# Optimization experiments

Hardware: AMD Instinct MI355X
Metric: run time of the kernel (lower is better)

Reference implementation:

```python
import jax, jax.numpy as jnp
import numpy as np

D = 256; NH = 8; HD = D // NH; FF = 1024; NLAYERS = 6
REG_MAX = 32; NBIN = REG_MAX + 1; NC = 80; KQ = 4
SPATIAL = [(80, 80), (40, 40), (20, 20)]; NPTS = [4, 4, 4]; SUMP = sum(NPTS)
LQ = 300; B = 16; OFFSET_SCALE = 0.5; UP = 0.5; REG_SCALE = 4.0
TOT = NH * SUMP


def _project_np():
    ub1 = abs(UP) * abs(REG_SCALE); ub2 = ub1 * 2
    step = (ub1 + 1.0) ** (2.0 / (REG_MAX - 2))
    left = [-(step ** i) + 1 for i in range(REG_MAX // 2 - 1, 0, -1)]
    right = [step ** i - 1 for i in range(1, REG_MAX // 2)]
    return np.array([-ub2] + left + [0.0] + right + [ub2], dtype=np.float32)

PROJ_NP = _project_np()  # [NBIN]


def layer_norm(x, g, b):
    mu = x.mean(-1, keepdims=True)
    var = ((x - mu) ** 2).mean(-1, keepdims=True)
    return (x - mu) * jax.lax.rsqrt(var + 1e-5) * g + b


def inv_sigmoid(x, eps=1e-5):
    x = jnp.clip(x, eps, 1.0 - eps)
    return jnp.log(x) - jnp.log1p(-x)


def mlp2(x, w1, b1, w2, b2):
    return jax.nn.silu(x @ w1 + b1) @ w2 + b2


def mlp3(x, w1, b1, w2, b2, w3, b3):
    return jax.nn.silu(jax.nn.silu(x @ w1 + b1) @ w2 + b2) @ w3 + b3


def grid_sample(img, grid):
    # bilinear, padding_mode='zeros', align_corners=False. img [N,C,H,W], grid [N,Hg,Wg,2] in [-1,1]
    N, C, H, W = img.shape
    gshape = grid.shape[1:3]
    x = (grid[..., 0] + 1.0) * (W * 0.5) - 0.5
    y = (grid[..., 1] + 1.0) * (H * 0.5) - 0.5
    x0f = jnp.floor(x); y0f = jnp.floor(y)
    wx = x - x0f; wy = y - y0f
    x0 = x0f.astype(jnp.int32); y0 = y0f.astype(jnp.int32)
    imgf = img.reshape(N, C, H * W)
    def tap(xi, yi, wt):
        valid = ((xi >= 0) & (xi < W) & (yi >= 0) & (yi < H)).astype(img.dtype)
        idx = jnp.clip(yi, 0, H - 1) * W + jnp.clip(xi, 0, W - 1)
        v = jnp.take_along_axis(imgf, idx.reshape(N, 1, -1), axis=2).reshape(N, C, gshape[0], gshape[1])
        return v * (valid * wt)[:, None]
    return (tap(x0, y0, (1 - wx) * (1 - wy)) + tap(x0 + 1, y0, wx * (1 - wy))
            + tap(x0, y0 + 1, (1 - wx) * wy) + tap(x0 + 1, y0 + 1, wx * wy))


def self_attention(q_in, k_in, v_in, qw, qb, kw, kb, vw, vb, ow, ob):
    q = (q_in @ qw + qb).reshape(B, LQ, NH, HD)
    k = (k_in @ kw + kb).reshape(B, LQ, NH, HD)
    v = (v_in @ vw + vb).reshape(B, LQ, NH, HD)
    a = jax.nn.softmax(jnp.einsum('bqhd,bkhd->bhqk', q, k) * (HD ** -0.5), -1)
    o = jnp.einsum('bhqk,bkhd->bqhd', a, v).reshape(B, LQ, D)
    return o @ ow + ob


def distance2bbox(points, distance):
    rs = abs(REG_SCALE); half = 0.5 * rs
    x1 = points[..., 0] - (half + distance[..., 0]) * (points[..., 2] / rs)
    y1 = points[..., 1] - (half + distance[..., 1]) * (points[..., 3] / rs)
    x2 = points[..., 0] + (half + distance[..., 2]) * (points[..., 2] / rs)
    y2 = points[..., 1] + (half + distance[..., 3]) * (points[..., 3] / rs)
    return jnp.stack([(x1 + x2) * 0.5, (y1 + y2) * 0.5, x2 - x1, y2 - y1], -1)


def lqe_head(scores, corners, w1, b1, w2, b2):
    prob = jax.nn.softmax(corners.reshape(B, LQ, 4, NBIN), -1)
    topk, _ = jax.lax.top_k(prob, KQ)                         # [B,LQ,4,KQ]
    stat = jnp.concatenate([topk, topk.mean(-1, keepdims=True)], -1)  # [B,LQ,4,KQ+1]
    return scores + mlp2(stat.reshape(B, LQ, 4 * (KQ + 1)), w1, b1, w2, b2)


def reference(target, ref_pts_unact, memory,
              sa_qw, sa_qb, sa_kw, sa_kb, sa_vw, sa_vb, sa_ow, sa_ob,
              n1_g, n1_b, off_w, off_b, aw_w, aw_b,
              gate_w, gate_b, gn_g, gn_b,
              ff1_w, ff1_b, ff2_w, ff2_b, n3_g, n3_b,
              bb_w1, bb_b1, bb_w2, bb_b2, bb_w3, bb_b3,
              sc_w, sc_b, lqe_w1, lqe_b1, lqe_w2, lqe_b2,
              qp_w1, qp_b1, qp_w2, qp_b2,
              pb_w1, pb_b1, pb_w2, pb_b2, pb_w3, pb_b3):
    project = jnp.asarray(PROJ_NP)
    # --- value prep: memory [B,S,D] -> per-level [B*NH, HD, h, w] ---
    val = memory.reshape(B, -1, NH, HD).transpose(0, 2, 3, 1).reshape(B * NH, HD, -1)
    splits = np.cumsum([h * w for h, w in SPATIAL])[:-1].tolist()
    value_lvls = [v.reshape(B * NH, HD, h, w)
                  for v, (h, w) in zip(jnp.split(val, splits, axis=2), SPATIAL)]
    nps = jnp.asarray(np.repeat(1.0 / np.array(NPTS, np.float32), NPTS))  # [SUMP]

    ref_pts = jax.nn.sigmoid(ref_pts_unact)
    output = target
    out_prev = jnp.zeros_like(target)
    corners_prev = jnp.zeros((B, LQ, 4 * NBIN), dtype=target.dtype)
    ref_init = ref_pts
    final_logits = final_bboxes = None

    for i in range(NLAYERS):
        qp = jnp.clip(mlp2(ref_pts, qp_w1, qp_b1, qp_w2, qp_b2), -10.0, 10.0)
        # self attention
        q = output + qp
        t2 = self_attention(q, q, output, sa_qw[i], sa_qb[i], sa_kw[i], sa_kb[i],
                            sa_vw[i], sa_vb[i], sa_ow[i], sa_ob[i])
        output = layer_norm(output + t2, n1_g[i], n1_b[i])
        # deformable cross attention
        qc = output + qp
        offs = (qc @ off_w[i] + off_b[i]).reshape(B, LQ, NH, SUMP, 2)
        attnw = jax.nn.softmax((qc @ aw_w[i] + aw_b[i]).reshape(B, LQ, NH, SUMP), -1)
        offset = offs * nps[:, None] * ref_pts[:, :, None, None, 2:] * OFFSET_SCALE
        locs = ref_pts[:, :, None, None, :2] + offset            # [B,LQ,NH,SUMP,2]
        grids = (2.0 * locs - 1.0).transpose(0, 2, 1, 3, 4).reshape(B * NH, LQ, SUMP, 2)
        p0 = 0; sampled = []
        for lvl in range(len(SPATIAL)):
            sampled.append(grid_sample(value_lvls[lvl], grids[:, :, p0:p0 + NPTS[lvl]]))
            p0 += NPTS[lvl]
        samp = jnp.concatenate(sampled, -1)                      # [B*NH, HD, LQ, SUMP]
        aw = attnw.transpose(0, 2, 1, 3).reshape(B * NH, 1, LQ, SUMP)
        t2 = (samp * aw).sum(-1).reshape(B, D, LQ).transpose(0, 2, 1)
        # gateway
        g12 = jax.nn.sigmoid(jnp.concatenate([output, t2], -1) @ gate_w[i] + gate_b[i])
        output = layer_norm(g12[..., :D] * output + g12[..., D:] * t2, gn_g[i], gn_b[i])
        # FFN
        t2 = jax.nn.relu(output @ ff1_w[i] + ff1_b[i]) @ ff2_w[i] + ff2_b[i]
        output = layer_norm(jnp.clip(output + t2, -65504.0, 65504.0), n3_g[i], n3_b[i])
        # FDR box refinement
        if i == 0:
            pre_bb = jax.nn.sigmoid(mlp3(output, pb_w1, pb_b1, pb_w2, pb_b2, pb_w3, pb_b3)
                                    + inv_sigmoid(ref_pts))
            ref_init = pre_bb
        corners = mlp3(output + out_prev, bb_w1[i], bb_b1[i], bb_w2[i], bb_b2[i],
                       bb_w3[i], bb_b3[i]) + corners_prev
        dist = jax.nn.softmax(corners.reshape(B, LQ, 4, NBIN), -1) @ project  # [B,LQ,4]
        inter = distance2bbox(ref_init, dist)
        if i == NLAYERS - 1:  # eval_idx
            scores = output @ sc_w[i] + sc_b[i]
            final_logits = lqe_head(scores, corners, lqe_w1[i], lqe_b1[i], lqe_w2[i], lqe_b2[i])
            final_bboxes = inter
        corners_prev = corners
        ref_pts = inter
        out_prev = output
    return jnp.concatenate([final_bboxes, final_logits], -1)  # [B, LQ, 4+NC]


def setup_inputs() -> dict:
    key = jax.random.key(0)
    cnt = [0]
    def rnd(shape, scale=0.02):
        cnt[0] += 1
        return jax.random.normal(jax.random.fold_in(key, cnt[0]), shape, dtype=jnp.float32) * scale
    S = sum(h * w for h, w in SPATIAL)
    L = NLAYERS
    return {
        'target': rnd((B, LQ, D), 1.0),
        'ref_pts_unact': rnd((B, LQ, 4), 1.0),
        'memory': rnd((B, S, D), 1.0),
        'sa_qw': rnd((L, D, D)), 'sa_qb': rnd((L, D)),
        'sa_kw': rnd((L, D, D)), 'sa_kb': rnd((L, D)),
        'sa_vw': rnd((L, D, D)), 'sa_vb': rnd((L, D)),
        'sa_ow': rnd((L, D, D)), 'sa_ob': rnd((L, D)),
        'n1_g': jnp.ones((L, D)), 'n1_b': jnp.zeros((L, D)),
        'off_w': rnd((L, D, TOT * 2)), 'off_b': rnd((L, TOT * 2)),
        'aw_w': rnd((L, D, TOT)), 'aw_b': rnd((L, TOT)),
        'gate_w': rnd((L, 2 * D, 2 * D)), 'gate_b': rnd((L, 2 * D)),
        'gn_g': jnp.ones((L, D)), 'gn_b': jnp.zeros((L, D)),
        'ff1_w': rnd((L, D, FF)), 'ff1_b': rnd((L, FF)),
        'ff2_w': rnd((L, FF, D)), 'ff2_b': rnd((L, D)),
        'n3_g': jnp.ones((L, D)), 'n3_b': jnp.zeros((L, D)),
        'bb_w1': rnd((L, D, D)), 'bb_b1': rnd((L, D)),
        'bb_w2': rnd((L, D, D)), 'bb_b2': rnd((L, D)),
        'bb_w3': rnd((L, D, 4 * NBIN)), 'bb_b3': rnd((L, 4 * NBIN)),
        'sc_w': rnd((L, D, NC)), 'sc_b': rnd((L, NC)),
        'lqe_w1': rnd((L, 4 * (KQ + 1), 64)), 'lqe_b1': rnd((L, 64)),
        'lqe_w2': rnd((L, 64, 1)), 'lqe_b2': rnd((L, 1)),
        'qp_w1': rnd((4, 2 * D)), 'qp_b1': rnd((2 * D,)),
        'qp_w2': rnd((2 * D, D)), 'qp_b2': rnd((D,)),
        'pb_w1': rnd((D, D)), 'pb_b1': rnd((D,)),
        'pb_w2': rnd((D, D)), 'pb_b2': rnd((D,)),
        'pb_w3': rnd((D, 4)), 'pb_b3': rnd((4,)),
    }
```

## Files before the change

kernel.cpp:

```cpp
#include <hip/hip_runtime.h>
#include <cstddef>
#include <cmath>
#include <utility>

#define B_ 16
#define LQ_ 300
#define D_ 256
#define NH_ 8
#define HD_ 32
#define FF_ 1024
#define NBIN_ 33
#define NC_ 80
#define SUMP_ 12
#define TOT_ (NH_*SUMP_)
#define STOT_ 8400
#define R_ (B_*LQ_)
#define NLAYERS_ 6

typedef short bf16x8 __attribute__((ext_vector_type(8)));
typedef float f32x4  __attribute__((ext_vector_type(4)));

static __device__ __forceinline__ short f2bf(float x) {
  union { float f; unsigned u; } v; v.f = x;
  unsigned r = v.u + 0x7fffu + ((v.u >> 16) & 1u);
  return (short)(r >> 16);
}
static __device__ __forceinline__ float bf2f(short s) {
  union { unsigned u; float f; } v; v.u = ((unsigned)(unsigned short)s) << 16; return v.f;
}

struct WJob { const float* src; short* dst; int K, N, tk, tn, L, ostride, blk0, pad; };
struct WJobs { WJob j[17]; int njobs; };

__launch_bounds__(256)
__global__ void wconv_all(WJobs P) {
  __shared__ float t[32][33];
  const int b = blockIdx.x;
  int ji = 0;
  for (int k = 1; k < P.njobs; ++k) ji = (b >= P.j[k].blk0) ? k : ji;
  const float* src = P.j[ji].src;
  short* dst = P.j[ji].dst;
  const int K = P.j[ji].K, N = P.j[ji].N, tk = P.j[ji].tk;
  int rel = b - P.j[ji].blk0;
  int per = tk * P.j[ji].tn;
  int l = rel / per; int r2 = rel - l * per;
  int tki = r2 % tk, tni = r2 / tk;
  const float* Wl = src + (size_t)l * K * N;
  short* Wtl = dst + (size_t)l * (size_t)P.j[ji].ostride;
  int k0 = tki * 32, n0 = tni * 32;
  int tr = threadIdx.x >> 5, tc = threadIdx.x & 31;
  #pragma unroll
  for (int i = 0; i < 4; ++i) {
    int k = k0 + tr + i * 8, n = n0 + tc;
    t[tr + i * 8][tc] = (k < K && n < N) ? Wl[(size_t)k * N + n] : 0.f;
  }
  __syncthreads();
  #pragma unroll
  for (int i = 0; i < 4; ++i) {
    int n = n0 + tr + i * 8, k = k0 + tc;
    if (n < N && k < K) Wtl[(size_t)n * K + k] = f2bf(t[tc][tr + i * 8]);
  }
}

__launch_bounds__(256)
__global__ void memconv_kernel(const float* __restrict__ mem, short* __restrict__ mb) {
  int gs = blockIdx.x * 4 + (threadIdx.x >> 6);
  int c  = (threadIdx.x & 63) * 4;
  int b = gs / STOT_, s = gs - b * STOT_;
  float4 v = *(const float4*)(mem + (size_t)gs * 256 + c);
  int h = c >> 5, cc = c & 31;
  short4 o; o.x = f2bf(v.x); o.y = f2bf(v.y); o.z = f2bf(v.z); o.w = f2bf(v.w);
  *(short4*)(mb + (((size_t)(b * 8 + h) * STOT_ + s) * 32) + cc) = o;
}

__launch_bounds__(256)
__global__ void misc_init(const float* __restrict__ target, const float* __restrict__ refu,
                          const float* __restrict__ qb, const float* __restrict__ kb,
                          const float* __restrict__ vb, const float* __restrict__ ob,
                          const float* __restrict__ ab,
                          float* __restrict__ output, short* __restrict__ outbf,
                          float* __restrict__ out_prev, float* __restrict__ cprev,
                          float* __restrict__ refcur, float* __restrict__ qkvb,
                          float* __restrict__ offawb) {
  int i = blockIdx.x * 256 + threadIdx.x;
  float4 z; z.x = 0.f; z.y = 0.f; z.z = 0.f; z.w = 0.f;
  if (i < R_ * 64) {
    float4 v = ((const float4*)target)[i];
    ((float4*)output)[i] = v;
    short4 s; s.x = f2bf(v.x); s.y = f2bf(v.y); s.z = f2bf(v.z); s.w = f2bf(v.w);
    ((short4*)outbf)[i] = s;
    ((float4*)out_prev)[i] = z;
  }
  if (i < R_ * 33) ((float4*)cprev)[i] = z;
  if (i < R_) {
    float4 r = ((const float4*)refu)[i];
    float4 o;
    o.x = 1.f / (1.f + __expf(-r.x)); o.y = 1.f / (1.f + __expf(-r.y));
    o.z = 1.f / (1.f + __expf(-r.z)); o.w = 1.f / (1.f + __expf(-r.w));
    ((float4*)refcur)[i] = o;
  }
  if (i < NLAYERS_ * 768) {
    int l = i / 768, c = i % 768;
    qkvb[i] = (c < 256) ? qb[l * 256 + c] : (c < 512) ? kb[l * 256 + c - 256]
                        : vb[l * 256 + c - 512];
  }
  if (i < NLAYERS_ * 288) {
    int l = i / 288, c = i % 288;
    offawb[i] = (c < 192) ? ob[l * 192 + c] : ab[l * 96 + c - 192];
  }
}

__launch_bounds__(512)
__global__ void qp_qkv(const float* __restrict__ ref, const float* __restrict__ W1,
                       const float* __restrict__ b1, const short* __restrict__ W2t,
                       const float* __restrict__ b2, const float* __restrict__ output,
                       const short* __restrict__ outbf,
                       const short* __restrict__ Qt, const float* __restrict__ qkvbias,
                       float* __restrict__ qpout, short* __restrict__ qkvout) {
  __shared__ short sh[16 * 520];
  __shared__ short oqs[16][264];
  const int m0 = blockIdx.x * 16;
  const int tid = threadIdx.x;
  for (int i = tid; i < 16 * 512; i += 512) {
    int r = i >> 9, n = i & 511;
    float4 rv = *(const float4*)(ref + (size_t)(m0 + r) * 4);
    float v = b1[n] + rv.x * W1[n] + rv.y * W1[512 + n] + rv.z * W1[1024 + n]
            + rv.w * W1[1536 + n];
    v = v / (1.f + __expf(-v));
    sh[r * 520 + n] = f2bf(v);
  }
  __syncthreads();
  const int wid = tid >> 6, lane = tid & 63;
  const int lr = lane & 15, lq = lane >> 4;
  {
    f32x4 acc[2];
    acc[0] = (f32x4){0.f, 0.f, 0.f, 0.f};
    acc[1] = (f32x4){0.f, 0.f, 0.f, 0.f};
    #pragma unroll 4
    for (int k0 = 0; k0 < 512; k0 += 32) {
      bf16x8 a = *(const bf16x8*)&sh[lr * 520 + k0 + lq * 8];
      #pragma unroll
      for (int t = 0; t < 2; ++t) {
        bf16x8 w = *(const bf16x8*)(W2t + (size_t)(wid * 32 + t * 16 + lr) * 512 + k0 + lq * 8);
        acc[t] = __builtin_amdgcn_mfma_f32_16x16x32_bf16(a, w, acc[t], 0, 0, 0);
      }
    }
    #pragma unroll
    for (int t = 0; t < 2; ++t) {
      int col = wid * 32 + t * 16 + lr;
      float bv = b2[col];
      #pragma unroll
      for (int rr = 0; rr < 4; ++rr) {
        int rl = lq * 4 + rr;
        size_t idx = (size_t)(m0 + rl) * 256 + col;
        float v = fminf(fmaxf(acc[t][rr] + bv, -10.f), 10.f);
        qpout[idx] = v;
        oqs[rl][col] = f2bf(v + output[idx]);
      }
    }
  }
  __syncthreads();
  {
    f32x4 acc[6];
    #pragma unroll
    for (int t = 0; t < 6; ++t) acc[t] = (f32x4){0.f, 0.f, 0.f, 0.f};
    const int cbase = wid * 96;
    const short* obp = outbf + (size_t)(m0 + lr) * 256;
    #pragma unroll 2
    for (int k0 = 0; k0 < 256; k0 += 32) {
      bf16x8 a_oq = *(const bf16x8*)&oqs[lr][k0 + lq * 8];
      bf16x8 a_ob = *(const bf16x8*)(obp + k0 + lq * 8);
      #pragma unroll
      for (int t = 0; t < 6; ++t) {
        bf16x8 w = *(const bf16x8*)(Qt + (size_t)(cbase + t * 16 + lr) * 256 + k0 + lq * 8);
        acc[t] = __builtin_amdgcn_mfma_f32_16x16x32_bf16(
            (cbase + t * 16 < 512) ? a_oq : a_ob, w, acc[t], 0, 0, 0);
      }
    }
    #pragma unroll
    for (int t = 0; t < 6; ++t) {
      int colt = cbase + t * 16 + lr;
      float bv = qkvbias[colt];
      #pragma unroll
      for (int rr = 0; rr < 4; ++rr)
        qkvout[(size_t)(m0 + lq * 4 + rr) * 768 + colt] = f2bf(acc[t][rr] + bv);
    }
  }
}

__launch_bounds__(512)
__global__ void sow_ln_off(const short* __restrict__ A, const short* __restrict__ Wt,
                           const float* __restrict__ bias, const float* __restrict__ resid,
                           const float* __restrict__ gamma, const float* __restrict__ beta,
                           const float* __restrict__ qp,
                           const short* __restrict__ OWt, const float* __restrict__ ob,
                           float* __restrict__ outf, short* __restrict__ outbf,
                           float* __restrict__ offout) {
  __shared__ float ssum[16][8];
  __shared__ float ssq[16][8];
  __shared__ short oqs[16][264];
  const int m0 = blockIdx.x * 16;
  const int tid = threadIdx.x, wid = tid >> 6, lane = tid & 63;
  const int lr = lane & 15, lq = lane >> 4;
  const int arow = m0 + lr;
  const int cw = wid * 32;
  f32x4 acc[2];
  acc[0] = (f32x4){0.f, 0.f, 0.f, 0.f};
  acc[1] = (f32x4){0.f, 0.f, 0.f, 0.f};
  #pragma unroll 4
  for (int k0 = 0; k0 < 256; k0 += 32) {
    bf16x8 a = *(const bf16x8*)(A + (size_t)arow * 256 + k0 + lq * 8);
    #pragma unroll
    for (int t = 0; t < 2; ++t) {
      bf16x8 w = *(const bf16x8*)(Wt + (size_t)(cw + t * 16 + lr) * 256 + k0 + lq * 8);
      acc[t] = __builtin_amdgcn_mfma_f32_16x16x32_bf16(a, w, acc[t], 0, 0, 0);
    }
  }
  float s[4] = {0.f, 0.f, 0.f, 0.f}, q[4] = {0.f, 0.f, 0.f, 0.f};
  #pragma unroll
  for (int t = 0; t < 2; ++t) {
    int col = cw + t * 16 + lr;
    float bv = bias[col];
    #pragma unroll
    for (int rr = 0; rr < 4; ++rr) {
      int rowg = m0 + lq * 4 + rr;
      float x = acc[t][rr] + bv + resid[(size_t)rowg * 256 + col];
      acc[t][rr] = x;
      s[rr] += x; q[rr] += x * x;
    }
  }
  #pragma unroll
  for (int m = 1; m < 16; m <<= 1)
    #pragma unroll
    for (int rr = 0; rr < 4; ++rr) { s[rr] += __shfl_xor(s[rr], m); q[rr] += __shfl_xor(q[rr], m); }
  if (lr == 0)
    #pragma unroll
    for (int rr = 0; rr < 4; ++rr) {
      ssum[lq * 4 + rr][wid] = s[rr];
      ssq[lq * 4 + rr][wid] = q[rr];
    }
  __syncthreads();
  float mu[4], rs[4];
  #pragma unroll
  for (int rr = 0; rr < 4; ++rr) {
    int rl = lq * 4 + rr;
    float sm = 0.f, sq = 0.f;
    #pragma unroll
    for (int w8 = 0; w8 < 8; ++w8) { sm += ssum[rl][w8]; sq += ssq[rl][w8]; }
    float m_ = sm * (1.f / 256.f);
    float var = sq * (1.f / 256.f) - m_ * m_;
    mu[rr] = m_; rs[rr] = rsqrtf(var + 1e-5f);
  }
  #pragma unroll
  for (int t = 0; t < 2; ++t) {
    int col = cw + t * 16 + lr;
    float g = gamma[col], be = beta[col];
    #pragma unroll
    for (int rr = 0; rr < 4; ++rr) {
      int rl = lq * 4 + rr;
      size_t idx = (size_t)(m0 + rl) * 256 + col;
      float v = (acc[t][rr] - mu[rr]) * rs[rr] * g + be;
      outf[idx] = v;
      outbf[idx] = f2bf(v);
      oqs[rl][col] = f2bf(v + qp[idx]);
    }
  }
  __syncthreads();
  f32x4 oacc[3];
  #pragma unroll
  for (int j = 0; j < 3; ++j) oacc[j] = (f32x4){0.f, 0.f, 0.f, 0.f};
  #pragma unroll 2
  for (int k0 = 0; k0 < 256; k0 += 32) {
    bf16x8 a = *(const bf16x8*)&oqs[lr][k0 + lq * 8];
    #pragma unroll
    for (int j = 0; j < 3; ++j) {
      int tile = wid + j * 8;
      int trow = (tile < 18) ? tile * 16 + lr : 0;
      bf16x8 w = *(const bf16x8*)(OWt + (size_t)trow * 256 + k0 + lq * 8);
      oacc[j] = __builtin_amdgcn_mfma_f32_16x16x32_bf16(a, w, oacc[j], 0, 0, 0);
    }
  }
  #pragma unroll
  for (int j = 0; j < 3; ++j) {
    int tile = wid + j * 8;
    if (tile >= 18) continue;
    int col = tile * 16 + lr;
    float bv = ob[col];
    #pragma unroll
    for (int rr = 0; rr < 4; ++rr)
      offout[(size_t)(m0 + lq * 4 + rr) * 288 + col] = oacc[j][rr] + bv;
  }
}

template<int SCORES>
__launch_bounds__(512)
__global__ void ffn_ln(const short* __restrict__ A, const short* __restrict__ W1t,
                       const float* __restrict__ b1, const short* __restrict__ W2t,
                       const float* __restrict__ b2, const float* __restrict__ resid,
                       const float* __restrict__ gamma, const float* __restrict__ beta,
                       float* __restrict__ prev, float* __restrict__ outf,
                       short* __restrict__ outbf, short* __restrict__ oqbf,
                       const short* __restrict__ SCt, const float* __restrict__ scb,
                       float* __restrict__ scoresOut) {
  __shared__ short hid[16][1032];
  __shared__ float ssum[16][8];
  __shared__ float ssq[16][8];
  const int m0 = blockIdx.x * 16;
  const int tid = threadIdx.x, wid = tid >> 6, lane = tid & 63;
  const int lr = lane & 15, lq = lane >> 4;
  const int arow = m0 + lr;
  {
    f32x4 acc[8];
    #pragma unroll
    for (int t = 0; t < 8; ++t) acc[t] = (f32x4){0.f, 0.f, 0.f, 0.f};
    #pragma unroll 2
    for (int k0 = 0; k0 < 256; k0 += 32) {
      bf16x8 a = *(const bf16x8*)(A + (size_t)arow * 256 + k0 + lq * 8);
      #pragma unroll
      for (int t = 0; t < 8; ++t) {
        bf16x8 w = *(const bf16x8*)(W1t + (size_t)(wid * 128 + t * 16 + lr) * 256 + k0 + lq * 8);
        acc[t] = __builtin_amdgcn_mfma_f32_16x16x32_bf16(a, w, acc[t], 0, 0, 0);
      }
    }
    #pragma unroll
    for (int t = 0; t < 8; ++t) {
      int col = wid * 128 + t * 16 + lr;
      float bv = b1[col];
      #pragma unroll
      for (int rr = 0; rr < 4; ++rr)
        hid[lq * 4 + rr][col] = f2bf(fmaxf(acc[t][rr] + bv, 0.f));
    }
  }
  __syncthreads();
  const int cw = wid * 32;
  f32x4 acc[2];
  acc[0] = (f32x4){0.f, 0.f, 0.f, 0.f};
  acc[1] = (f32x4){0.f, 0.f, 0.f, 0.f};
  #pragma unroll 4
  for (int k0 = 0; k0 < 1024; k0 += 32) {
    bf16x8 a = *(const bf16x8*)&hid[lr][k0 + lq * 8];
    #pragma unroll
    for (int t = 0; t < 2; ++t) {
      bf16x8 w = *(const bf16x8*)(W2t + (size_t)(cw + t * 16 + lr) * 1024 + k0 + lq * 8);
      acc[t] = __builtin_amdgcn_mfma_f32_16x16x32_bf16(a, w, acc[t], 0, 0, 0);
    }
  }
  float s[4] = {0.f, 0.f, 0.f, 0.f}, q[4] = {0.f, 0.f, 0.f, 0.f};
  #pragma unroll
  for (int t = 0; t < 2; ++t) {
    int col = cw + t * 16 + lr;
    float bv = b2[col];
    #pragma unroll
    for (int rr = 0; rr < 4; ++rr) {
      int rowg = m0 + lq * 4 + rr;
      float x = acc[t][rr] + bv + resid[(size_t)rowg * 256 + col];
      x = fminf(fmaxf(x, -65504.f), 65504.f);
      acc[t][rr] = x;
      s[rr] += x; q[rr] += x * x;
    }
  }
  #pragma unroll
  for (int m = 1; m < 16; m <<= 1)
    #pragma unroll
    for (int rr = 0; rr < 4; ++rr) { s[rr] += __shfl_xor(s[rr], m); q[rr] += __shfl_xor(q[rr], m); }
  if (lr == 0)
    #pragma unroll
    for (int rr = 0; rr < 4; ++rr) {
      ssum[lq * 4 + rr][wid] = s[rr];
      ssq[lq * 4 + rr][wid] = q[rr];
    }
  __syncthreads();
  float mu[4], rs[4];
  #pragma unroll
  for (int rr = 0; rr < 4; ++rr) {
    int rl = lq * 4 + rr;
    float sm = 0.f, sq = 0.f;
    #pragma unroll
    for (int w8 = 0; w8 < 8; ++w8) { sm += ssum[rl][w8]; sq += ssq[rl][w8]; }
    float m_ = sm * (1.f / 256.f);
    float var = sq * (1.f / 256.f) - m_ * m_;
    mu[rr] = m_; rs[rr] = rsqrtf(var + 1e-5f);
  }
  #pragma unroll
  for (int t = 0; t < 2; ++t) {
    int col = cw + t * 16 + lr;
    float g = gamma[col], be = beta[col];
    #pragma unroll
    for (int rr = 0; rr < 4; ++rr) {
      int rl = lq * 4 + rr;
      size_t idx = (size_t)(m0 + rl) * 256 + col;
      float v = (acc[t][rr] - mu[rr]) * rs[rr] * g + be;
      outf[idx] = v;
      short vb = f2bf(v);
      outbf[idx] = vb;
      float po = prev[idx];
      oqbf[idx] = f2bf(v + po);
      prev[idx] = v;
      if (SCORES) hid[rl][col] = vb;
    }
  }
  if (SCORES) {
    __syncthreads();
    f32x4 sacc = (f32x4){0.f, 0.f, 0.f, 0.f};
    int trow = (wid < 5) ? wid * 16 + lr : 0;
    #pragma unroll 2
    for (int k0 = 0; k0 < 256; k0 += 32) {
      bf16x8 a = *(const bf16x8*)&hid[lr][k0 + lq * 8];
      bf16x8 w = *(const bf16x8*)(SCt + (size_t)trow * 256 + k0 + lq * 8);
      sacc = __builtin_amdgcn_mfma_f32_16x16x32_bf16(a, w, sacc, 0, 0, 0);
    }
    if (wid < 5) {
      int col = wid * 16 + lr;
      float bv = scb[col];
      #pragma unroll
      for (int rr = 0; rr < 4; ++rr)
        scoresOut[(size_t)(m0 + lq * 4 + rr) * 80 + col] = sacc[rr] + bv;
    }
  }
}

template<int LQE>
__launch_bounds__(512)
__global__ void fdr_kernel(const short* __restrict__ A,
                           const short* __restrict__ W1t, const float* __restrict__ b1,
                           const short* __restrict__ W2t, const float* __restrict__ b2,
                           const short* __restrict__ W3t, const float* __restrict__ b3,
                           const float* __restrict__ cprev, const float* __restrict__ refi,
                           float* __restrict__ ccur, float* __restrict__ refn,
                           const float* __restrict__ scores, const float* __restrict__ lw1,
                           const float* __restrict__ lb1, const float* __restrict__ lw2,
                           const float* __restrict__ lb2, float* __restrict__ outp) {
  __shared__ short h1[16][264];
  __shared__ short h2[16][264];
  __shared__ float cor[16][132];
  __shared__ float dstl[16][4];
  __shared__ float projs[33];
  __shared__ float statl[16][20];
  __shared__ float interb[16][4];
  __shared__ float lqes[16];
  const int m0 = blockIdx.x * 16;
  const int tid = threadIdx.x, wid = tid >> 6, lane = tid & 63;
  const int lr = lane & 15, lq = lane >> 4;
  if (tid < 33) {
    float v;
    if (tid == 0) v = -4.f;
    else if (tid == 32) v = 4.f;
    else if (tid == 16) v = 0.f;
    else if (tid < 16) v = 1.f - powf(3.f, (float)(16 - tid) * (1.f / 15.f));
    else v = powf(3.f, (float)(tid - 16) * (1.f / 15.f)) - 1.f;
    projs[tid] = v;
  }
  {
    f32x4 acc[2];
    acc[0] = (f32x4){0.f, 0.f, 0.f, 0.f};
    acc[1] = (f32x4){0.f, 0.f, 0.f, 0.f};
    #pragma unroll 2
    for (int k0 = 0; k0 < 256; k0 += 32) {
      bf16x8 a = *(const bf16x8*)(A + (size_t)(m0 + lr) * 256 + k0 + lq * 8);
      #pragma unroll
      for (int t = 0; t < 2; ++t) {
        bf16x8 w = *(const bf16x8*)(W1t + (size_t)(wid * 32 + t * 16 + lr) * 256 + k0 + lq * 8);
        acc[t] = __builtin_amdgcn_mfma_f32_16x16x32_bf16(a, w, acc[t], 0, 0, 0);
      }
    }
    #pragma unroll
    for (int t = 0; t < 2; ++t) {
      int col = wid * 32 + t * 16 + lr;
      float bv = b1[col];
      #pragma unroll
      for (int rr = 0; rr < 4; ++rr) {
        float v = acc[t][rr] + bv;
        v = v / (1.f + __expf(-v));
        h1[lq * 4 + rr][col] = f2bf(v);
      }
    }
  }
  __syncthreads();
  {
    f32x4 acc[2];
    acc[0] = (f32x4){0.f, 0.f, 0.f, 0.f};
    acc[1] = (f32x4){0.f, 0.f, 0.f, 0.f};
    #pragma unroll 2
    for (int k0 = 0; k0 < 256; k0 += 32) {
      bf16x8 a = *(const bf16x8*)&h1[lr][k0 + lq * 8];
      #pragma unroll
      for (int t = 0; t < 2; ++t) {
        bf16x8 w = *(const bf16x8*)(W2t + (size_t)(wid * 32 + t * 16 + lr) * 256 + k0 + lq * 8);
        acc[t] = __builtin_amdgcn_mfma_f32_16x16x32_bf16(a, w, acc[t], 0, 0, 0);
      }
    }
    #pragma unroll
    for (int t = 0; t < 2; ++t) {
      int col = wid * 32 + t * 16 + lr;
      float bv = b2[col];
      #pragma unroll
      for (int rr = 0; rr < 4; ++rr) {
        float v = acc[t][rr] + bv;
        v = v / (1.f + __expf(-v));
        h2[lq * 4 + rr][col] = f2bf(v);
      }
    }
  }
  __syncthreads();
  {
    f32x4 acc[2];
    int col[2], wr[2];
    #pragma unroll
    for (int j = 0; j < 2; ++j) {
      acc[j] = (f32x4){0.f, 0.f, 0.f, 0.f};
      col[j] = (wid + j * 8) * 16 + lr;
      wr[j] = (col[j] < 132) ? col[j] : 0;
    }
    #pragma unroll 2
    for (int k0 = 0; k0 < 256; k0 += 32) {
      bf16x8 a = *(const bf16x8*)&h2[lr][k0 + lq * 8];
      #pragma unroll
      for (int j = 0; j < 2; ++j) {
        bf16x8 w = *(const bf16x8*)(W3t + (size_t)wr[j] * 256 + k0 + lq * 8);
        acc[j] = __builtin_amdgcn_mfma_f32_16x16x32_bf16(a, w, acc[j], 0, 0, 0);
      }
    }
    #pragma unroll
    for (int j = 0; j < 2; ++j) {
      if (col[j] >= 132) continue;
      float bv = b3[col[j]];
      #pragma unroll
      for (int rr = 0; rr < 4; ++rr) {
        int rl = lq * 4 + rr, g = m0 + rl;
        float v = acc[j][rr] + bv + cprev[(size_t)g * 132 + col[j]];
        ccur[(size_t)g * 132 + col[j]] = v;
        cor[rl][col[j]] = v;
      }
    }
  }
  __syncthreads();
  if (tid < 64) {
    int r = tid >> 2, sd = tid & 3;
    const float* cp = &cor[r][sd * 33];
    float m = -1e30f;
    #pragma unroll
    for (int j = 0; j < 33; ++j) m = fmaxf(m, cp[j]);
    float t0 = -1e30f, t1 = -1e30f, t2v = -1e30f, t3 = -1e30f;
    float sum = 0.f, dot = 0.f;
    #pragma unroll
    for (int j = 0; j < 33; ++j) {
      float e = __expf(cp[j] - m);
      sum += e; dot += e * projs[j];
      if (LQE) {
        if (e > t0)      { t3 = t2v; t2v = t1; t1 = t0; t0 = e; }
        else if (e > t1) { t3 = t2v; t2v = t1; t1 = e; }
        else if (e > t2v){ t3 = t2v; t2v = e; }
        else if (e > t3) { t3 = e; }
      }
    }
    dstl[r][sd] = dot / sum;
    if (LQE) {
      float inv = 1.f / sum;
      float v0 = t0 * inv, v1 = t1 * inv, v2 = t2v * inv, v3 = t3 * inv;
      statl[r][sd * 5 + 0] = v0; statl[r][sd * 5 + 1] = v1;
      statl[r][sd * 5 + 2] = v2; statl[r][sd * 5 + 3] = v3;
      statl[r][sd * 5 + 4] = (v0 + v1 + v2 + v3) * 0.25f;
    }
  }
  __syncthreads();
  if (tid < 16) {
    int g = m0 + tid;
    float px = refi[g * 4], py = refi[g * 4 + 1];
    float qw = refi[g * 4 + 2] * 0.25f, qh = refi[g * 4 + 3] * 0.25f;
    float x1 = px - (2.f + dstl[tid][0]) * qw, y1 = py - (2.f + dstl[tid][1]) * qh;
    float x2 = px + (2.f + dstl[tid][2]) * qw, y2 = py + (2.f + dstl[tid][3]) * qh;
    float4 o; o.x = (x1 + x2) * 0.5f; o.y = (y1 + y2) * 0.5f; o.z = x2 - x1; o.w = y2 - y1;
    *(float4*)(refn + (size_t)g * 4) = o;
    if (LQE) { interb[tid][0] = o.x; interb[tid][1] = o.y; interb[tid][2] = o.z; interb[tid][3] = o.w; }
  }
  if (LQE) {
    #pragma unroll
    for (int it = 0; it < 2; ++it) {
      int row = wid * 2 + it;
      float sv = lb1[lane];
      #pragma unroll
      for (int i = 0; i < 20; ++i) sv += statl[row][i] * lw1[i * 64 + lane];
      float hv = sv / (1.f + __expf(-sv));
      float v = hv * lw2[lane];
      #pragma unroll
      for (int o = 32; o; o >>= 1) v += __shfl_xor(v, o);
      if (lane == 0) lqes[row] = v + lb2[0];
    }
    __syncthreads();
    for (int idx = tid; idx < 16 * 84; idx += 512) {
      int r = idx / 84, c = idx - r * 84;
      int g = m0 + r;
      outp[(size_t)g * 84 + c] = (c < 4) ? interb[r][c]
                                         : scores[(size_t)g * 80 + (c - 4)] + lqes[r];
    }
  }
}

__launch_bounds__(512)
__global__ void pb_fused(const short* __restrict__ A,
                         const short* __restrict__ W1t, const float* __restrict__ b1,
                         const short* __restrict__ W2t, const float* __restrict__ b2,
                         const short* __restrict__ W3t, const float* __restrict__ b3,
                         const float* __restrict__ refc, float* __restrict__ refinit) {
  __shared__ short h1[16][264];
  __shared__ short h2[16][264];
  const int m0 = blockIdx.x * 16;
  const int tid = threadIdx.x, wid = tid >> 6, lane = tid & 63;
  const int lr = lane & 15, lq = lane >> 4;
  {
    f32x4 acc[2];
    acc[0] = (f32x4){0.f, 0.f, 0.f, 0.f};
    acc[1] = (f32x4){0.f, 0.f, 0.f, 0.f};
    #pragma unroll 2
    for (int k0 = 0; k0 < 256; k0 += 32) {
      bf16x8 a = *(const bf16x8*)(A + (size_t)(m0 + lr) * 256 + k0 + lq * 8);
      #pragma unroll
      for (int t = 0; t < 2; ++t) {
        bf16x8 w = *(const bf16x8*)(W1t + (size_t)(wid * 32 + t * 16 + lr) * 256 + k0 + lq * 8);
        acc[t] = __builtin_amdgcn_mfma_f32_16x16x32_bf16(a, w, acc[t], 0, 0, 0);
      }
    }
    #pragma unroll
    for (int t = 0; t < 2; ++t) {
      int col = wid * 32 + t * 16 + lr;
      float bv = b1[col];
      #pragma unroll
      for (int rr = 0; rr < 4; ++rr) {
        float v = acc[t][rr] + bv;
        v = v / (1.f + __expf(-v));
        h1[lq * 4 + rr][col] = f2bf(v);
      }
    }
  }
  __syncthreads();
  {
    f32x4 acc[2];
    acc[0] = (f32x4){0.f, 0.f, 0.f, 0.f};
    acc[1] = (f32x4){0.f, 0.f, 0.f, 0.f};
    #pragma unroll 2
    for (int k0 = 0; k0 < 256; k0 += 32) {
      bf16x8 a = *(const bf16x8*)&h1[lr][k0 + lq * 8];
      #pragma unroll
      for (int t = 0; t < 2; ++t) {
        bf16x8 w = *(const bf16x8*)(W2t + (size_t)(wid * 32 + t * 16 + lr) * 256 + k0 + lq * 8);
        acc[t] = __builtin_amdgcn_mfma_f32_16x16x32_bf16(a, w, acc[t], 0, 0, 0);
      }
    }
    #pragma unroll
    for (int t = 0; t < 2; ++t) {
      int col = wid * 32 + t * 16 + lr;
      float bv = b2[col];
      #pragma unroll
      for (int rr = 0; rr < 4; ++rr) {
        float v = acc[t][rr] + bv;
        v = v / (1.f + __expf(-v));
        h2[lq * 4 + rr][col] = f2bf(v);
      }
    }
  }
  __syncthreads();
  if (wid == 0) {
    f32x4 acc = (f32x4){0.f, 0.f, 0.f, 0.f};
    const short* wp = W3t + (size_t)((lr < 4) ? lr : 0) * 256;
    #pragma unroll 2
    for (int k0 = 0; k0 < 256; k0 += 32) {
      bf16x8 a = *(const bf16x8*)&h2[lr][k0 + lq * 8];
      bf16x8 w = *(const bf16x8*)(wp + k0 + lq * 8);
      acc = __builtin_amdgcn_mfma_f32_16x16x32_bf16(a, w, acc, 0, 0, 0);
    }
    if (lr < 4) {
      float bv = b3[lr];
      #pragma unroll
      for (int rr = 0; rr < 4; ++rr) {
        int g = m0 + lq * 4 + rr;
        float pre = acc[rr] + bv;
        float x = fminf(fmaxf(refc[(size_t)g * 4 + lr], 1e-5f), 1.f - 1e-5f);
        float is = logf(x) - log1pf(-x);
        refinit[(size_t)g * 4 + lr] = 1.f / (1.f + __expf(-(pre + is)));
      }
    }
  }
}

__launch_bounds__(512)
__global__ void gate_ln(const short* __restrict__ Abf, const short* __restrict__ tbf,
                        const short* __restrict__ Wt, const float* __restrict__ bias,
                        const float* __restrict__ t2,
                        const float* __restrict__ gamma, const float* __restrict__ beta,
                        float* __restrict__ output, short* __restrict__ outbf) {
  __shared__ float sg[16][520];
  const int m0 = blockIdx.x * 16;
  const int tid = threadIdx.x, wid = tid >> 6, lane = tid & 63;
  const int lr = lane & 15, lq = lane >> 4;
  const int arow = m0 + lr;
  f32x4 acc[4];
  #pragma unroll
  for (int t = 0; t < 4; ++t) acc[t] = (f32x4){0.f, 0.f, 0.f, 0.f};
  #pragma unroll 2
  for (int k0 = 0; k0 < 512; k0 += 32) {
    const short* src = (k0 < 256) ? Abf : tbf;
    int ko = (k0 < 256) ? k0 : k0 - 256;
    bf16x8 a = *(const bf16x8*)(src + (size_t)arow * 256 + ko + lq * 8);
    #pragma unroll
    for (int t = 0; t < 4; ++t) {
      bf16x8 w = *(const bf16x8*)(Wt + (size_t)(wid * 64 + t * 16 + lr) * 512 + k0 + lq * 8);
      acc[t] = __builtin_amdgcn_mfma_f32_16x16x32_bf16(a, w, acc[t], 0, 0, 0);
    }
  }
  #pragma unroll
  for (int t = 0; t < 4; ++t) {
    int col = wid * 64 + t * 16 + lr;
    float bv = bias[col];
    #pragma unroll
    for (int rr = 0; rr < 4; ++rr) {
      int rl = lq * 4 + rr;
      sg[rl][col] = 1.f / (1.f + __expf(-(acc[t][rr] + bv)));
    }
  }
  __syncthreads();
  #pragma unroll
  for (int it = 0; it < 2; ++it) {
    int rl = wid + it * 8;
    int rowg = m0 + rl;
    int c = lane * 4;
    float4 o4 = *(const float4*)(output + (size_t)rowg * 256 + c);
    float4 t4 = *(const float4*)(t2 + (size_t)rowg * 256 + c);
    float4 g1 = *(const float4*)&sg[rl][c];
    float4 g2 = *(const float4*)&sg[rl][256 + c];
    float x0 = g1.x * o4.x + g2.x * t4.x;
    float x1 = g1.y * o4.y + g2.y * t4.y;
    float x2 = g1.z * o4.z + g2.z * t4.z;
    float x3 = g1.w * o4.w + g2.w * t4.w;
    float s = x0 + x1 + x2 + x3;
    float q = x0 * x0 + x1 * x1 + x2 * x2 + x3 * x3;
    #pragma unroll
    for (int o = 32; o; o >>= 1) { s += __shfl_xor(s, o); q += __shfl_xor(q, o); }
    float mu = s * (1.f / 256.f);
    float var = q * (1.f / 256.f) - mu * mu;
    float rs = rsqrtf(var + 1e-5f);
    float4 ga = *(const float4*)(gamma + c);
    float4 be = *(const float4*)(beta + c);
    float v0 = (x0 - mu) * rs * ga.x + be.x;
    float v1 = (x1 - mu) * rs * ga.y + be.y;
    float v2 = (x2 - mu) * rs * ga.z + be.z;
    float v3 = (x3 - mu) * rs * ga.w + be.w;
    float4 vo; vo.x = v0; vo.y = v1; vo.z = v2; vo.w = v3;
    *(float4*)(output + (size_t)rowg * 256 + c) = vo;
    short4 vs; vs.x = f2bf(v0); vs.y = f2bf(v1); vs.z = f2bf(v2); vs.w = f2bf(v3);
    *(short4*)(outbf + (size_t)rowg * 256 + c) = vs;
  }
}

__launch_bounds__(256)
__global__ void attn3_kernel(const short* __restrict__ qkv, short* __restrict__ O) {
  __shared__ short Kb[304][40];
  __shared__ short Vt[32][328];
  __shared__ short Pw[4][16][328];
  const int half = blockIdx.x & 1, bh = blockIdx.x >> 1;
  const int h = bh & 7, b = bh >> 3;
  const int tid = threadIdx.x;
  const short* QKVb = qkv + (size_t)b * LQ_ * 768;
  for (int idx = tid; idx < 304 * 4; idx += 256) {
    int row = idx >> 2, seg = (idx & 3) * 8;
    bf16x8 v = (row < 300) ? *(const bf16x8*)(QKVb + (size_t)row * 768 + 256 + h * 32 + seg)
                           : (bf16x8){0,0,0,0,0,0,0,0};
    *(bf16x8*)&Kb[row][seg] = v;
  }
  for (int idx = tid; idx < 300 * 4; idx += 256) {
    int row = idx >> 2, seg = (idx & 3) * 8;
    bf16x8 v = *(const bf16x8*)(QKVb + (size_t)row * 768 + 512 + h * 32 + seg);
    #pragma unroll
    for (int j = 0; j < 8; ++j) Vt[seg + j][row] = v[j];
  }
  for (int idx = tid; idx < 32 * 20; idx += 256) Vt[idx / 20][300 + idx % 20] = 0;
  for (int idx = tid; idx < 4 * 16 * 16; idx += 256)
    Pw[idx >> 8][(idx >> 4) & 15][304 + (idx & 15)] = 0;
  __syncthreads();

  const int wid = tid >> 6, lane = tid & 63;
  const int lr = lane & 15, lq = lane >> 4;
  short (*Pl)[328] = Pw[wid];
  const float scale = 0.17677669529663687f;

  for (int qt = wid; qt < 10; qt += 4) {
    const int q0 = half * 150 + qt * 16;
    int qrow = q0 + lr; if (qrow > 299) qrow = 299;
    bf16x8 af_q = *(const bf16x8*)(QKVb + (size_t)qrow * 768 + h * 32 + lq * 8);
    f32x4 s[19];
    #pragma unroll
    for (int t = 0; t < 19; ++t) {
      bf16x8 bk = *(const bf16x8*)&Kb[t * 16 + lr][lq * 8];
      s[t] = __builtin_amdgcn_mfma_f32_16x16x32_bf16(af_q, bk, (f32x4){0.f,0.f,0.f,0.f}, 0, 0, 0);
    }
    #pragma unroll
    for (int t = 0; t < 19; ++t)
      #pragma unroll
      for (int r = 0; r < 4; ++r) s[t][r] *= scale;
    if (lr >= 12) { s[18][0] = s[18][1] = s[18][2] = s[18][3] = -1e30f; }
    float l[4];
    #pragma unroll
    for (int r = 0; r < 4; ++r) {
      float mm = -1e30f;
      #pragma unroll
      for (int t = 0; t < 19; ++t) mm = fmaxf(mm, s[t][r]);
      #pragma unroll
      for (int x = 1; x < 16; x <<= 1) mm = fmaxf(mm, __shfl_xor(mm, x));
      float ll = 0.f;
      #pragma unroll
      for (int t = 0; t < 19; ++t) { float p = __expf(s[t][r] - mm); s[t][r] = p; ll += p; }
      #pragma unroll
      for (int x = 1; x < 16; x <<= 1) ll += __shfl_xor(ll, x);
      l[r] = ll;
    }
    #pragma unroll
    for (int t = 0; t < 19; ++t)
      #pragma unroll
      for (int r = 0; r < 4; ++r) Pl[lq * 4 + r][t * 16 + lr] = f2bf(s[t][r]);
    f32x4 o0 = (f32x4){0.f,0.f,0.f,0.f}, o1 = (f32x4){0.f,0.f,0.f,0.f};
    #pragma unroll
    for (int c = 0; c < 10; ++c) {
      bf16x8 ap = *(const bf16x8*)&Pl[lr][c * 32 + lq * 8];
      bf16x8 v0 = *(const bf16x8*)&Vt[lr][c * 32 + lq * 8];
      bf16x8 v1 = *(const bf16x8*)&Vt[16 + lr][c * 32 + lq * 8];
      o0 = __builtin_amdgcn_mfma_f32_16x16x32_bf16(ap, v0, o0, 0, 0, 0);
      o1 = __builtin_amdgcn_mfma_f32_16x16x32_bf16(ap, v1, o1, 0, 0, 0);
    }
    #pragma unroll
    for (int r = 0; r < 4; ++r) {
      int q = q0 + lq * 4 + r;
      if (q >= 300) continue;
      float inv = 1.f / l[r];
      size_t ob = (size_t)(b * LQ_ + q) * 256 + h * 32;
      O[ob + lr]      = f2bf(o0[r] * inv);
      O[ob + 16 + lr] = f2bf(o1[r] * inv);
    }
  }
}

template<int BF16MEM>
__launch_bounds__(256)
__global__ void deform_kernel(const void* __restrict__ memv, const float* __restrict__ offaw,
                              const float* __restrict__ refp,
                              float* __restrict__ t2, short* __restrict__ t2bf) {
  const int bi = blockIdx.x;
  const int row = (bi & 7) * 600 + (bi >> 3);
  const int b = row / LQ_;
  const int tid = threadIdx.x;
  const int h = tid >> 5, c = tid & 31;
  const float rx = refp[row * 4 + 0], ry = refp[row * 4 + 1];
  const float rw = refp[row * 4 + 2], rh = refp[row * 4 + 3];
  const float* awp = offaw + (size_t)row * 288 + 192 + h * SUMP_;
  float wv[SUMP_];
  float wmax = -1e30f;
  #pragma unroll
  for (int p = 0; p < SUMP_; ++p) { wv[p] = awp[p]; wmax = fmaxf(wmax, wv[p]); }
  float wsum = 0.f;
  #pragma unroll
  for (int p = 0; p < SUMP_; ++p) { wv[p] = __expf(wv[p] - wmax); wsum += wv[p]; }
  const float winv = 1.f / wsum;
  const float* op = offaw + (size_t)row * 288 + h * (SUMP_ * 2);
  const short* mb16 = BF16MEM ? ((const short*)memv + ((size_t)(b * 8 + h) * STOT_) * 32 + c) : nullptr;
  const float* mb32 = BF16MEM ? nullptr : ((const float*)memv + (size_t)b * STOT_ * 256 + h * 32 + c);
  float acc = 0.f;
  #pragma unroll
  for (int p = 0; p < SUMP_; ++p) {
    const int lvl = p >> 2;
    const int Wl = (lvl == 0) ? 80 : ((lvl == 1) ? 40 : 20);
    const int s0 = (lvl == 0) ? 0 : ((lvl == 1) ? 6400 : 8000);
    float lx = rx + op[2 * p]     * 0.125f * rw;
    float ly = ry + op[2 * p + 1] * 0.125f * rh;
    float x = lx * Wl - 0.5f, y = ly * Wl - 0.5f;
    float xf = floorf(x), yf = floorf(y);
    int x0 = (int)xf, y0 = (int)yf;
    float wx = x - xf, wy = y - yf;
    int x0c = min(max(x0, 0), Wl - 1), x1c = min(max(x0 + 1, 0), Wl - 1);
    int y0c = min(max(y0, 0), Wl - 1), y1c = min(max(y0 + 1, 0), Wl - 1);
    float wx0 = (x0 >= 0 && x0 < Wl) ? (1.f - wx) : 0.f;
    float wx1 = (x0 + 1 >= 0 && x0 + 1 < Wl) ? wx : 0.f;
    float wy0 = (y0 >= 0 && y0 < Wl) ? (1.f - wy) : 0.f;
    float wy1 = (y0 + 1 >= 0 && y0 + 1 < Wl) ? wy : 0.f;
    float v;
    if (BF16MEM) {
      const short* mb = mb16 + (size_t)s0 * 32;
      v = wx0 * wy0 * bf2f(mb[(size_t)(y0c * Wl + x0c) * 32])
        + wx1 * wy0 * bf2f(mb[(size_t)(y0c * Wl + x1c) * 32])
        + wx0 * wy1 * bf2f(mb[(size_t)(y1c * Wl + x0c) * 32])
        + wx1 * wy1 * bf2f(mb[(size_t)(y1c * Wl + x1c) * 32]);
    } else {
      const float* mb = mb32 + (size_t)s0 * 256;
      v = wx0 * wy0 * mb[(size_t)(y0c * Wl + x0c) * 256]
        + wx1 * wy0 * mb[(size_t)(y0c * Wl + x1c) * 256]
        + wx0 * wy1 * mb[(size_t)(y1c * Wl + x0c) * 256]
        + wx1 * wy1 * mb[(size_t)(y1c * Wl + x1c) * 256];
    }
    acc += wv[p] * winv * v;
  }
  size_t off = (size_t)row * D_ + h * HD_ + c;
  t2[off] = acc;
  t2bf[off] = f2bf(acc);
}

static inline dim3 egrid(int n) { return dim3((n + 255) / 256); }

extern "C" void kernel_launch(void* const* d_in, const int* in_sizes, int n_in,
                              void* d_out, int out_size, void* d_ws, size_t ws_size,
                              hipStream_t stream) {
  const float* target     = (const float*)d_in[0];
  const float* ref_unact  = (const float*)d_in[1];
  const float* memory     = (const float*)d_in[2];
  const float* sa_qw = (const float*)d_in[3];  const float* sa_qb = (const float*)d_in[4];
  const float* sa_kw = (const float*)d_in[5];  const float* sa_kb = (const float*)d_in[6];
  const float* sa_vw = (const float*)d_in[7];  const float* sa_vb = (const float*)d_in[8];
  const float* sa_ow = (const float*)d_in[9];  const float* sa_ob = (const float*)d_in[10];
  const float* n1_g  = (const float*)d_in[11]; const float* n1_b  = (const float*)d_in[12];
  const float* off_w = (const float*)d_in[13]; const float* off_b = (const float*)d_in[14];
  const float* aw_w  = (const float*)d_in[15]; const float* aw_b  = (const float*)d_in[16];
  const float* gate_w= (const float*)d_in[17]; const float* gate_b= (const float*)d_in[18];
  const float* gn_g  = (const float*)d_in[19]; const float* gn_b  = (const float*)d_in[20];
  const float* ff1_w = (const float*)d_in[21]; const float* ff1_b = (const float*)d_in[22];
  const float* ff2_w = (const float*)d_in[23]; const float* ff2_b = (const float*)d_in[24];
  const float* n3_g  = (const float*)d_in[25]; const float* n3_b  = (const float*)d_in[26];
  const float* bb_w1 = (const float*)d_in[27]; const float* bb_b1 = (const float*)d_in[28];
  const float* bb_w2 = (const float*)d_in[29]; const float* bb_b2 = (const float*)d_in[30];
  const float* bb_w3 = (const float*)d_in[31]; const float* bb_b3 = (const float*)d_in[32];
  const float* sc_w  = (const float*)d_in[33]; const float* sc_b  = (const float*)d_in[34];
  const float* lqe_w1= (const float*)d_in[35]; const float* lqe_b1= (const float*)d_in[36];
  const float* lqe_w2= (const float*)d_in[37]; const float* lqe_b2= (const float*)d_in[38];
  const float* qp_w1 = (const float*)d_in[39]; const float* qp_b1 = (const float*)d_in[40];
  const float* qp_w2 = (const float*)d_in[41]; const float* qp_b2 = (const float*)d_in[42];
  const float* pb_w1 = (const float*)d_in[43]; const float* pb_b1 = (const float*)d_in[44];
  const float* pb_w2 = (const float*)d_in[45]; const float* pb_b2 = (const float*)d_in[46];
  const float* pb_w3 = (const float*)d_in[47]; const float* pb_b3 = (const float*)d_in[48];
  float* out = (float*)d_out;

  float* ws = (float*)d_ws;
  size_t woff = 0;
  auto alloc = [&](size_t n) { float* p = ws + woff; woff += n; return p; };
  float* output   = alloc((size_t)R_ * D_);
  float* out_prev = alloc((size_t)R_ * D_);
  float* qp       = alloc((size_t)R_ * D_);
  float* t2       = alloc((size_t)R_ * D_);
  float* offawf   = alloc((size_t)R_ * 288);
  float* U        = alloc((size_t)R_ * 512);
  float* corners0 = alloc((size_t)R_ * 4 * NBIN_);
  float* corners1 = alloc((size_t)R_ * 4 * NBIN_);
  float* refA     = alloc((size_t)R_ * 4);
  float* refB     = alloc((size_t)R_ * 4);
  float* ref_init = alloc((size_t)R_ * 4);
  float* qkvb     = alloc((size_t)NLAYERS_ * 768);
  float* offawb   = alloc((size_t)NLAYERS_ * 288);

  short* sws = (short*)(ws + woff);
  size_t soff = 0;
  auto salloc = [&](size_t n) { short* p = sws + soff; soff += n; return p; };
  short* outbf = salloc((size_t)R_ * D_);
  short* oqbf  = salloc((size_t)R_ * D_);
  short* tbf   = salloc((size_t)R_ * D_);
  short* qp2t  = salloc((size_t)256 * 512);
  short* sqkvt = salloc((size_t)NLAYERS_ * 768 * 256);
  short* sowt  = salloc((size_t)NLAYERS_ * 256 * 256);
  short* soffawt = salloc((size_t)NLAYERS_ * 288 * 256);
  short* gatet = salloc((size_t)NLAYERS_ * 512 * 512);
  short* ff1t  = salloc((size_t)NLAYERS_ * 1024 * 256);
  short* ff2t  = salloc((size_t)NLAYERS_ * 256 * 1024);
  short* bb1t  = salloc((size_t)NLAYERS_ * 256 * 256);
  short* bb2t  = salloc((size_t)NLAYERS_ * 256 * 256);
  short* bb3t  = salloc((size_t)NLAYERS_ * 132 * 256);
  short* pb1t  = salloc((size_t)256 * 256);
  short* pb2t  = salloc((size_t)256 * 256);
  short* pb3t  = salloc((size_t)4 * 256);
  short* sct   = salloc((size_t)80 * 256);
  size_t base_bytes = woff * sizeof(float) + soff * sizeof(short);
  if (ws_size < base_bytes) return;
  const size_t memn = (size_t)B_ * STOT_ * 256;
  bool bf16mem = (ws_size >= base_bytes + memn * sizeof(short));
  short* membf = sws + soff;

  short* qkv    = (short*)U;
  float* scores = offawf;

  float* c_prev = corners0; float* c_cur = corners1;
  float* ref_cur = refA;    float* ref_nxt = refB;

  WJobs P; int nb = 0; int nj = 0;
  auto addj = [&](const float* s, short* d2, int K, int N, int L, int ostr) {
    P.j[nj].src = s; P.j[nj].dst = d2; P.j[nj].K = K; P.j[nj].N = N;
    P.j[nj].tk = (K + 31) / 32; P.j[nj].tn = (N + 31) / 32;
    P.j[nj].L = L; P.j[nj].ostride = ostr; P.j[nj].blk0 = nb; P.j[nj].pad = 0;
    nb += P.j[nj].tk * P.j[nj].tn * L; ++nj;
  };
  addj(qp_w2, qp2t, 512, 256, 1, 512 * 256);
  addj(sa_qw, sqkvt,               256, 256, NLAYERS_, 768 * 256);
  addj(sa_kw, sqkvt + 256 * 256,   256, 256, NLAYERS_, 768 * 256);
  addj(sa_vw, sqkvt + 512 * 256,   256, 256, NLAYERS_, 768 * 256);
  addj(sa_ow, sowt, 256, 256, NLAYERS_, 256 * 256);
  addj(off_w, soffawt,             256, 192, NLAYERS_, 288 * 256);
  addj(aw_w,  soffawt + 192 * 256, 256,  96, NLAYERS_, 288 * 256);
  addj(gate_w, gatet, 512, 512, NLAYERS_, 512 * 512);
  addj(ff1_w, ff1t, 256, 1024, NLAYERS_, 1024 * 256);
  addj(ff2_w, ff2t, 1024, 256, NLAYERS_, 256 * 1024);
  addj(bb_w1, bb1t, 256, 256, NLAYERS_, 256 * 256);
  addj(bb_w2, bb2t, 256, 256, NLAYERS_, 256 * 256);
  addj(bb_w3, bb3t, 256, 132, NLAYERS_, 132 * 256);
  addj(pb_w1, pb1t, 256, 256, 1, 256 * 256);
  addj(pb_w2, pb2t, 256, 256, 1, 256 * 256);
  addj(pb_w3, pb3t, 256, 4, 1, 4 * 256);
  addj(sc_w + (size_t)5 * D_ * NC_, sct, 256, 80, 1, 80 * 256);
  P.njobs = nj;
  wconv_all<<<dim3(nb), 256, 0, stream>>>(P);
  if (bf16mem)
    memconv_kernel<<<dim3(B_ * STOT_ / 4), 256, 0, stream>>>(memory, membf);

  misc_init<<<egrid(R_ * 64), 256, 0, stream>>>(target, ref_unact,
      sa_qb, sa_kb, sa_vb, off_b, aw_b,
      output, outbf, out_prev, c_prev, ref_cur, qkvb, offawb);

  for (int i = 0; i < NLAYERS_; ++i) {
    qp_qkv<<<dim3(300), 512, 0, stream>>>(ref_cur, qp_w1, qp_b1, qp2t, qp_b2,
                                          output, outbf,
                                          sqkvt + (size_t)i * 768 * 256,
                                          qkvb + (size_t)i * 768, qp, qkv);
    attn3_kernel<<<dim3(B_ * NH_ * 2), 256, 0, stream>>>(qkv, tbf);
    sow_ln_off<<<dim3(300), 512, 0, stream>>>(
        tbf, sowt + (size_t)i * 65536, sa_ob + (size_t)i * D_, output,
        n1_g + (size_t)i * D_, n1_b + (size_t)i * D_, qp,
        soffawt + (size_t)i * 288 * 256, offawb + (size_t)i * 288,
        output, outbf, offawf);

    if (bf16mem)
      deform_kernel<1><<<dim3(R_), 256, 0, stream>>>(membf, offawf, ref_cur, t2, tbf);
    else
      deform_kernel<0><<<dim3(R_), 256, 0, stream>>>(memory, offawf, ref_cur, t2, tbf);

    gate_ln<<<dim3(300), 512, 0, stream>>>(outbf, tbf, gatet + (size_t)i * 262144,
                                           gate_b + (size_t)i * 512, t2,
                                           gn_g + (size_t)i * D_, gn_b + (size_t)i * D_,
                                           output, outbf);

    if (i < NLAYERS_ - 1)
      ffn_ln<0><<<dim3(300), 512, 0, stream>>>(outbf, ff1t + (size_t)i * 262144,
          ff1_b + (size_t)i * FF_, ff2t + (size_t)i * 262144, ff2_b + (size_t)i * D_,
          output, n3_g + (size_t)i * D_, n3_b + (size_t)i * D_,
          out_prev, output, outbf, oqbf, nullptr, nullptr, nullptr);
    else
      ffn_ln<1><<<dim3(300), 512, 0, stream>>>(outbf, ff1t + (size_t)i * 262144,
          ff1_b + (size_t)i * FF_, ff2t + (size_t)i * 262144, ff2_b + (size_t)i * D_,
          output, n3_g + (size_t)i * D_, n3_b + (size_t)i * D_,
          out_prev, output, outbf, oqbf, sct, sc_b + (size_t)5 * NC_, scores);

    if (i == 0)
      pb_fused<<<dim3(300), 512, 0, stream>>>(outbf, pb1t, pb_b1, pb2t, pb_b2,
                                              pb3t, pb_b3, ref_cur, ref_init);
    if (i < NLAYERS_ - 1) {
      fdr_kernel<0><<<dim3(300), 512, 0, stream>>>(oqbf,
          bb1t + (size_t)i * 65536, bb_b1 + (size_t)i * D_,
          bb2t + (size_t)i * 65536, bb_b2 + (size_t)i * D_,
          bb3t + (size_t)i * 33792, bb_b3 + (size_t)i * 4 * NBIN_,
          c_prev, ref_init, c_cur, ref_nxt,
          nullptr, nullptr, nullptr, nullptr, nullptr, nullptr);
      std::swap(c_prev, c_cur);
      std::swap(ref_cur, ref_nxt);
    } else {
      fdr_kernel<1><<<dim3(300), 512, 0, stream>>>(oqbf,
          bb1t + (size_t)i * 65536, bb_b1 + (size_t)i * D_,
          bb2t + (size_t)i * 65536, bb_b2 + (size_t)i * D_,
          bb3t + (size_t)i * 33792, bb_b3 + (size_t)i * 4 * NBIN_,
          c_prev, ref_init, c_cur, ref_nxt,
          scores, lqe_w1 + (size_t)5 * 20 * 64, lqe_b1 + (size_t)5 * 64,
          lqe_w2 + (size_t)5 * 64, lqe_b2 + (size_t)5, out);
    }
  }
}
```

Measured before the change: 1.885 ms.

## Double row tile to 32 per block across fused GEMM kernels

Every fused MFMA kernel (qp_qkv, sow_ln_off, ffn_ln, gate_ln, pb_fused, fdr) now handles 32 rows per block instead of 16. Each weight fragment is reused for two A tiles, which halves global weight traffic per row. Grids drop from 300 to 150 blocks. The deform kernel also packs two rows per 512-thread block. The tradeoff is fewer blocks than the MI355X's CU count (256), more registers and LDS per block, and lower occupancy.

Result: faster. 1.607 ms (-14.8%).

```diff
diff --git a/kernel.cpp b/kernel.cpp
--- a/kernel.cpp
+++ b/kernel.cpp
@@ -117,11 +117,11 @@
                        const short* __restrict__ outbf,
                        const short* __restrict__ Qt, const float* __restrict__ qkvbias,
                        float* __restrict__ qpout, short* __restrict__ qkvout) {
-  __shared__ short sh[16 * 520];
-  __shared__ short oqs[16][264];
-  const int m0 = blockIdx.x * 16;
+  __shared__ short sh[32 * 520];
+  __shared__ short oqs[32][264];
+  const int m0 = blockIdx.x * 32;
   const int tid = threadIdx.x;
-  for (int i = tid; i < 16 * 512; i += 512) {
+  for (int i = tid; i < 32 * 512; i += 512) {
     int r = i >> 9, n = i & 511;
     float4 rv = *(const float4*)(ref + (size_t)(m0 + r) * 4);
     float v = b1[n] + rv.x * W1[n] + rv.y * W1[512 + n] + rv.z * W1[1024 + n]
@@ -133,16 +133,20 @@
   const int wid = tid >> 6, lane = tid & 63;
   const int lr = lane & 15, lq = lane >> 4;
   {
-    f32x4 acc[2];
-    acc[0] = (f32x4){0.f, 0.f, 0.f, 0.f};
-    acc[1] = (f32x4){0.f, 0.f, 0.f, 0.f};
+    f32x4 acc[2][2];
+    #pragma unroll
+    for (int ti = 0; ti < 2; ++ti)
+      #pragma unroll
+      for (int t = 0; t < 2; ++t) acc[ti][t] = (f32x4){0.f, 0.f, 0.f, 0.f};
     #pragma unroll 4
     for (int k0 = 0; k0 < 512; k0 += 32) {
-      bf16x8 a = *(const bf16x8*)&sh[lr * 520 + k0 + lq * 8];
+      bf16x8 a0 = *(const bf16x8*)&sh[lr * 520 + k0 + lq * 8];
+      bf16x8 a1 = *(const bf16x8*)&sh[(16 + lr) * 520 + k0 + lq * 8];
       #pragma unroll
       for (int t = 0; t < 2; ++t) {
         bf16x8 w = *(const bf16x8*)(W2t + (size_t)(wid * 32 + t * 16 + lr) * 512 + k0 + lq * 8);
-        acc[t] = __builtin_amdgcn_mfma_f32_16x16x32_bf16(a, w, acc[t], 0, 0, 0);
+        acc[0][t] = __builtin_amdgcn_mfma_f32_16x16x32_bf16(a0, w, acc[0][t], 0, 0, 0);
+        acc[1][t] = __builtin_amdgcn_mfma_f32_16x16x32_bf16(a1, w, acc[1][t], 0, 0, 0);
       }
     }
     #pragma unroll
@@ -150,31 +154,39 @@
       int col = wid * 32 + t * 16 + lr;
       float bv = b2[col];
       #pragma unroll
-      for (int rr = 0; rr < 4; ++rr) {
-        int rl = lq * 4 + rr;
-        size_t idx = (size_t)(m0 + rl) * 256 + col;
-        float v = fminf(fmaxf(acc[t][rr] + bv, -10.f), 10.f);
-        qpout[idx] = v;
-        oqs[rl][col] = f2bf(v + output[idx]);
-      }
+      for (int ti = 0; ti < 2; ++ti)
+        #pragma unroll
+        for (int rr = 0; rr < 4; ++rr) {
+          int rl = ti * 16 + lq * 4 + rr;
+          size_t idx = (size_t)(m0 + rl) * 256 + col;
+          float v = fminf(fmaxf(acc[ti][t][rr] + bv, -10.f), 10.f);
+          qpout[idx] = v;
+          oqs[rl][col] = f2bf(v + output[idx]);
+        }
     }
   }
   __syncthreads();
   {
-    f32x4 acc[6];
-    #pragma unroll
-    for (int t = 0; t < 6; ++t) acc[t] = (f32x4){0.f, 0.f, 0.f, 0.f};
+    f32x4 acc[2][6];
+    #pragma unroll
+    for (int ti = 0; ti < 2; ++ti)
+      #pragma unroll
+      for (int t = 0; t < 6; ++t) acc[ti][t] = (f32x4){0.f, 0.f, 0.f, 0.f};
     const int cbase = wid * 96;
-    const short* obp = outbf + (size_t)(m0 + lr) * 256;
+    const short* obp0 = outbf + (size_t)(m0 + lr) * 256;
+    const short* obp1 = outbf + (size_t)(m0 + 16 + lr) * 256;
     #pragma unroll 2
     for (int k0 = 0; k0 < 256; k0 += 32) {
-      bf16x8 a_oq = *(const bf16x8*)&oqs[lr][k0 + lq * 8];
-      bf16x8 a_ob = *(const bf16x8*)(obp + k0 + lq * 8);
+      bf16x8 aq0 = *(const bf16x8*)&oqs[lr][k0 + lq * 8];
+      bf16x8 aq1 = *(const bf16x8*)&oqs[16 + lr][k0 + lq * 8];
+      bf16x8 ab0 = *(const bf16x8*)(obp0 + k0 + lq * 8);
+      bf16x8 ab1 = *(const bf16x8*)(obp1 + k0 + lq * 8);
       #pragma unroll
       for (int t = 0; t < 6; ++t) {
         bf16x8 w = *(const bf16x8*)(Qt + (size_t)(cbase + t * 16 + lr) * 256 + k0 + lq * 8);
-        acc[t] = __builtin_amdgcn_mfma_f32_16x16x32_bf16(
-            (cbase + t * 16 < 512) ? a_oq : a_ob, w, acc[t], 0, 0, 0);
+        bool useoq = (cbase + t * 16) < 512;
+        acc[0][t] = __builtin_amdgcn_mfma_f32_16x16x32_bf16(useoq ? aq0 : ab0, w, acc[0][t], 0, 0, 0);
+        acc[1][t] = __builtin_amdgcn_mfma_f32_16x16x32_bf16(useoq ? aq1 : ab1, w, acc[1][t], 0, 0, 0);
       }
     }
     #pragma unroll
@@ -182,8 +194,10 @@
       int colt = cbase + t * 16 + lr;
       float bv = qkvbias[colt];
       #pragma unroll
-      for (int rr = 0; rr < 4; ++rr)
-        qkvout[(size_t)(m0 + lq * 4 + rr) * 768 + colt] = f2bf(acc[t][rr] + bv);
+      for (int ti = 0; ti < 2; ++ti)
+        #pragma unroll
+        for (int rr = 0; rr < 4; ++rr)
+          qkvout[(size_t)(m0 + ti * 16 + lq * 4 + rr) * 768 + colt] = f2bf(acc[ti][t][rr] + bv);
     }
   }
 }
@@ -196,88 +210,112 @@
                            const short* __restrict__ OWt, const float* __restrict__ ob,
                            float* __restrict__ outf, short* __restrict__ outbf,
                            float* __restrict__ offout) {
-  __shared__ float ssum[16][8];
-  __shared__ float ssq[16][8];
-  __shared__ short oqs[16][264];
-  const int m0 = blockIdx.x * 16;
+  __shared__ float ssum[32][8];
+  __shared__ float ssq[32][8];
+  __shared__ short oqs[32][264];
+  const int m0 = blockIdx.x * 32;
   const int tid = threadIdx.x, wid = tid >> 6, lane = tid & 63;
   const int lr = lane & 15, lq = lane >> 4;
-  const int arow = m0 + lr;
   const int cw = wid * 32;
-  f32x4 acc[2];
-  acc[0] = (f32x4){0.f, 0.f, 0.f, 0.f};
-  acc[1] = (f32x4){0.f, 0.f, 0.f, 0.f};
+  f32x4 acc[2][2];
+  #pragma unroll
+  for (int ti = 0; ti < 2; ++ti)
+    #pragma unroll
+    for (int t = 0; t < 2; ++t) acc[ti][t] = (f32x4){0.f, 0.f, 0.f, 0.f};
   #pragma unroll 4
   for (int k0 = 0; k0 < 256; k0 += 32) {
-    bf16x8 a = *(const bf16x8*)(A + (size_t)arow * 256 + k0 + lq * 8);
+    bf16x8 a0 = *(const bf16x8*)(A + (size_t)(m0 + lr) * 256 + k0 + lq * 8);
+    bf16x8 a1 = *(const bf16x8*)(A + (size_t)(m0 + 16 + lr) * 256 + k0 + lq * 8);
     #pragma unroll
     for (int t = 0; t < 2; ++t) {
       bf16x8 w = *(const bf16x8*)(Wt + (size_t)(cw + t * 16 + lr) * 256 + k0 + lq * 8);
-      acc[t] = __builtin_amdgcn_mfma_f32_16x16x32_bf16(a, w, acc[t], 0, 0, 0);
-    }
-  }
-  float s[4] = {0.f, 0.f, 0.f, 0.f}, q[4] = {0.f, 0.f, 0.f, 0.f};
+      acc[0][t] = __builtin_amdgcn_mfma_f32_16x16x32_bf16(a0, w, acc[0][t], 0, 0, 0);
+      acc[1][t] = __builtin_amdgcn_mfma_f32_16x16x32_bf16(a1, w, acc[1][t], 0, 0, 0);
+    }
+  }
+  float s[2][4], q[2][4];
+  #pragma unroll
+  for (int ti = 0; ti < 2; ++ti)
+    #pragma unroll
+    for (int rr = 0; rr < 4; ++rr) { s[ti][rr] = 0.f; q[ti][rr] = 0.f; }
   #pragma unroll
   for (int t = 0; t < 2; ++t) {
     int col = cw + t * 16 + lr;
     float bv = bias[col];
     #pragma unroll
+    for (int ti = 0; ti < 2; ++ti)
+      #pragma unroll
+      for (int rr = 0; rr < 4; ++rr) {
+        int rowg = m0 + ti * 16 + lq * 4 + rr;
+        float x = acc[ti][t][rr] + bv + resid[(size_t)rowg * 256 + col];
+        acc[ti][t][rr] = x;
+        s[ti][rr] += x; q[ti][rr] += x * x;
+      }
+  }
+  #pragma unroll
+  for (int m = 1; m < 16; m <<= 1)
+    #pragma unroll
+    for (int ti = 0; ti < 2; ++ti)
+      #pragma unroll
+      for (int rr = 0; rr < 4; ++rr) {
+        s[ti][rr] += __shfl_xor(s[ti][rr], m);
+        q[ti][rr] += __shfl_xor(q[ti][rr], m);
+      }
+  if (lr == 0)
+    #pragma unroll
+    for (int ti = 0; ti < 2; ++ti)
+      #pragma unroll
+      for (int rr = 0; rr < 4; ++rr) {
+        ssum[ti * 16 + lq * 4 + rr][wid] = s[ti][rr];
+        ssq[ti * 16 + lq * 4 + rr][wid] = q[ti][rr];
+      }
+  __syncthreads();
+  float mu[2][4], rs[2][4];
+  #pragma unroll
+  for (int ti = 0; ti < 2; ++ti)
+    #pragma unroll
     for (int rr = 0; rr < 4; ++rr) {
-      int rowg = m0 + lq * 4 + rr;
-      float x = acc[t][rr] + bv + resid[(size_t)rowg * 256 + col];
-      acc[t][rr] = x;
-      s[rr] += x; q[rr] += x * x;
-    }
-  }
-  #pragma unroll
-  for (int m = 1; m < 16; m <<= 1)
-    #pragma unroll
-    for (int rr = 0; rr < 4; ++rr) { s[rr] += __shfl_xor(s[rr], m); q[rr] += __shfl_xor(q[rr], m); }
-  if (lr == 0)
-    #pragma unroll
-    for (int rr = 0; rr < 4; ++rr) {
-      ssum[lq * 4 + rr][wid] = s[rr];
-      ssq[lq * 4 + rr][wid] = q[rr];
-    }
-  __syncthreads();
-  float mu[4], rs[4];
-  #pragma unroll
-  for (int rr = 0; rr < 4; ++rr) {
-    int rl = lq * 4 + rr;
-    float sm = 0.f, sq = 0.f;
-    #pragma unroll
-    for (int w8 = 0; w8 < 8; ++w8) { sm += ssum[rl][w8]; sq += ssq[rl][w8]; }
-    float m_ = sm * (1.f / 256.f);
-    float var = sq * (1.f / 256.f) - m_ * m_;
-    mu[rr] = m_; rs[rr] = rsqrtf(var + 1e-5f);
-  }
+      int rl = ti * 16 + lq * 4 + rr;
+      float sm = 0.f, sq = 0.f;
+      #pragma unroll
+      for (int w8 = 0; w8 < 8; ++w8) { sm += ssum[rl][w8]; sq += ssq[rl][w8]; }
+      float m_ = sm * (1.f / 256.f);
+      float var = sq * (1.f / 256.f) - m_ * m_;
+      mu[ti][rr] = m_; rs[ti][rr] = rsqrtf(var + 1e-5f);
+    }
   #pragma unroll
   for (int t = 0; t < 2; ++t) {
     int col = cw + t * 16 + lr;
     float g = gamma[col], be = beta[col];
     #pragma unroll
-    for (int rr = 0; rr < 4; ++rr) {
-      int rl = lq * 4 + rr;
-      size_t idx = (size_t)(m0 + rl) * 256 + col;
-      float v = (acc[t][rr] - mu[rr]) * rs[rr] * g + be;
-      outf[idx] = v;
-      outbf[idx] = f2bf(v);
-      oqs[rl][col] = f2bf(v + qp[idx]);
-    }
-  }
-  __syncthreads();
-  f32x4 oacc[3];
-  #pragma unroll
-  for (int j = 0; j < 3; ++j) oacc[j] = (f32x4){0.f, 0.f, 0.f, 0.f};
+    for (int ti = 0; ti < 2; ++ti)
+      #pragma unroll
+      for (int rr = 0; rr < 4; ++rr) {
+        int rl = ti * 16 + lq * 4 + rr;
+        size_t idx = (size_t)(m0 + rl) * 256 + col;
+        float v = (acc[ti][t][rr] - mu[ti][rr]) * rs[ti][rr] * g + be;
+        outf[idx] = v;
+        outbf[idx] = f2bf(v);
+        oqs[rl][col] = f2bf(v + qp[idx]);
+      }
+  }
+  __syncthreads();
+  f32x4 oacc[2][3];
+  #pragma unroll
+  for (int ti = 0; ti < 2; ++ti)
+    #pragma unroll
+    for (int j = 0; j < 3; ++j) oacc[ti][j] = (f32x4){0.f, 0.f, 0.f, 0.f};
   #pragma unroll 2
   for (int k0 = 0; k0 < 256; k0 += 32) {
-    bf16x8 a = *(const bf16x8*)&oqs[lr][k0 + lq * 8];
+    bf16x8 a0 = *(const bf16x8*)&oqs[lr][k0 + lq * 8];
+    bf16x8 a1 = *(const bf16x8*)&oqs[16 + lr][k0 + lq * 8];
     #pragma unroll
     for (int j = 0; j < 3; ++j) {
       int tile = wid + j * 8;
       int trow = (tile < 18) ? tile * 16 + lr : 0;
       bf16x8 w = *(const bf16x8*)(OWt + (size_t)trow * 256 + k0 + lq * 8);
-      oacc[j] = __builtin_amdgcn_mfma_f32_16x16x32_bf16(a, w, oacc[j], 0, 0, 0);
+      oacc[0][j] = __builtin_amdgcn_mfma_f32_16x16x32_bf16(a0, w, oacc[0][j], 0, 0, 0);
+      oacc[1][j] = __builtin_amdgcn_mfma_f32_16x16x32_bf16(a1, w, oacc[1][j], 0, 0, 0);
     }
   }
   #pragma unroll
@@ -287,8 +325,10 @@
     int col = tile * 16 + lr;
     float bv = ob[col];
     #pragma unroll
-    for (int rr = 0; rr < 4; ++rr)
-      offout[(size_t)(m0 + lq * 4 + rr) * 288 + col] = oacc[j][rr] + bv;
+    for (int ti = 0; ti < 2; ++ti)
+      #pragma unroll
+      for (int rr = 0; rr < 4; ++rr)
+        offout[(size_t)(m0 + ti * 16 + lq * 4 + rr) * 288 + col] = oacc[ti][j][rr] + bv;
   }
 }
 
@@ -302,24 +342,27 @@
                        short* __restrict__ outbf, short* __restrict__ oqbf,
                        const short* __restrict__ SCt, const float* __restrict__ scb,
                        float* __restrict__ scoresOut) {
-  __shared__ short hid[16][1032];
-  __shared__ float ssum[16][8];
-  __shared__ float ssq[16][8];
-  const int m0 = blockIdx.x * 16;
+  __shared__ short hid[32][1032];
+  __shared__ float ssum[32][8];
+  __shared__ float ssq[32][8];
+  const int m0 = blockIdx.x * 32;
   const int tid = threadIdx.x, wid = tid >> 6, lane = tid & 63;
   const int lr = lane & 15, lq = lane >> 4;
-  const int arow = m0 + lr;
   {
-    f32x4 acc[8];
-    #pragma unroll
-    for (int t = 0; t < 8; ++t) acc[t] = (f32x4){0.f, 0.f, 0.f, 0.f};
+    f32x4 acc[2][8];
+    #pragma unroll
+    for (int ti = 0; ti < 2; ++ti)
+      #pragma unroll
+      for (int t = 0; t < 8; ++t) acc[ti][t] = (f32x4){0.f, 0.f, 0.f, 0.f};
     #pragma unroll 2
     for (int k0 = 0; k0 < 256; k0 += 32) {
-      bf16x8 a = *(const bf16x8*)(A + (size_t)arow * 256 + k0 + lq * 8);
+      bf16x8 a0 = *(const bf16x8*)(A + (size_t)(m0 + lr) * 256 + k0 + lq * 8);
+      bf16x8 a1 = *(const bf16x8*)(A + (size_t)(m0 + 16 + lr) * 256 + k0 + lq * 8);
       #pragma unroll
       for (int t = 0; t < 8; ++t) {
         bf16x8 w = *(const bf16x8*)(W1t + (size_t)(wid * 128 + t * 16 + lr) * 256 + k0 + lq * 8);
-        acc[t] = __builtin_amdgcn_mfma_f32_16x16x32_bf16(a, w, acc[t], 0, 0, 0);
+        acc[0][t] = __builtin_amdgcn_mfma_f32_16x16x32_bf16(a0, w, acc[0][t], 0, 0, 0);
+        acc[1][t] = __builtin_amdgcn_mfma_f32_16x16x32_bf16(a1, w, acc[1][t], 0, 0, 0);
       }
     }
     #pragma unroll
@@ -327,94 +370,123 @@
       int col = wid * 128 + t * 16 + lr;
       float bv = b1[col];
       #pragma unroll
-      for (int rr = 0; rr < 4; ++rr)
-        hid[lq * 4 + rr][col] = f2bf(fmaxf(acc[t][rr] + bv, 0.f));
+      for (int ti = 0; ti < 2; ++ti)
+        #pragma unroll
+        for (int rr = 0; rr < 4; ++rr)
+          hid[ti * 16 + lq * 4 + rr][col] = f2bf(fmaxf(acc[ti][t][rr] + bv, 0.f));
     }
   }
   __syncthreads();
   const int cw = wid * 32;
-  f32x4 acc[2];
-  acc[0] = (f32x4){0.f, 0.f, 0.f, 0.f};
-  acc[1] = (f32x4){0.f, 0.f, 0.f, 0.f};
+  f32x4 acc[2][2];
+  #pragma unroll
+  for (int ti = 0; ti < 2; ++ti)
+    #pragma unroll
+    for (int t = 0; t < 2; ++t) acc[ti][t] = (f32x4){0.f, 0.f, 0.f, 0.f};
   #pragma unroll 4
   for (int k0 = 0; k0 < 1024; k0 += 32) {
-    bf16x8 a = *(const bf16x8*)&hid[lr][k0 + lq * 8];
+    bf16x8 a0 = *(const bf16x8*)&hid[lr][k0 + lq * 8];
+    bf16x8 a1 = *(const bf16x8*)&hid[16 + lr][k0 + lq * 8];
     #pragma unroll
     for (int t = 0; t < 2; ++t) {
       bf16x8 w = *(const bf16x8*)(W2t + (size_t)(cw + t * 16 + lr) * 1024 + k0 + lq * 8);
-      acc[t] = __builtin_amdgcn_mfma_f32_16x16x32_bf16(a, w, acc[t], 0, 0, 0);
-    }
-  }
-  float s[4] = {0.f, 0.f, 0.f, 0.f}, q[4] = {0.f, 0.f, 0.f, 0.f};
+      acc[0][t] = __builtin_amdgcn_mfma_f32_16x16x32_bf16(a0, w, acc[0][t], 0, 0, 0);
+      acc[1][t] = __builtin_amdgcn_mfma_f32_16x16x32_bf16(a1, w, acc[1][t], 0, 0, 0);
+    }
+  }
+  float s[2][4], q[2][4];
+  #pragma unroll
+  for (int ti = 0; ti < 2; ++ti)
+    #pragma unroll
+    for (int rr = 0; rr < 4; ++rr) { s[ti][rr] = 0.f; q[ti][rr] = 0.f; }
   #pragma unroll
   for (int t = 0; t < 2; ++t) {
     int col = cw + t * 16 + lr;
     float bv = b2[col];
     #pragma unroll
+    for (int ti = 0; ti < 2; ++ti)
+      #pragma unroll
+      for (int rr = 0; rr < 4; ++rr) {
+        int rowg = m0 + ti * 16 + lq * 4 + rr;
+        float x = acc[ti][t][rr] + bv + resid[(size_t)rowg * 256 + col];
+        x = fminf(fmaxf(x, -65504.f), 65504.f);
+        acc[ti][t][rr] = x;
+        s[ti][rr] += x; q[ti][rr] += x * x;
+      }
+  }
+  #pragma unroll
+  for (int m = 1; m < 16; m <<= 1)
+    #pragma unroll
+    for (int ti = 0; ti < 2; ++ti)
+      #pragma unroll
+      for (int rr = 0; rr < 4; ++rr) {
+        s[ti][rr] += __shfl_xor(s[ti][rr], m);
+        q[ti][rr] += __shfl_xor(q[ti][rr], m);
+      }
+  if (lr == 0)
+    #pragma unroll
+    for (int ti = 0; ti < 2; ++ti)
+      #pragma unroll
+      for (int rr = 0; rr < 4; ++rr) {
+        ssum[ti * 16 + lq * 4 + rr][wid] = s[ti][rr];
+        ssq[ti * 16 + lq * 4 + rr][wid] = q[ti][rr];
+      }
+  __syncthreads();
+  float mu[2][4], rs[2][4];
+  #pragma unroll
+  for (int ti = 0; ti < 2; ++ti)
+    #pragma unroll
     for (int rr = 0; rr < 4; ++rr) {
-      int rowg = m0 + lq * 4 + rr;
-      float x = acc[t][rr] + bv + resid[(size_t)rowg * 256 + col];
-      x = fminf(fmaxf(x, -65504.f), 65504.f);
-      acc[t][rr] = x;
-      s[rr] += x; q[rr] += x * x;
-    }
-  }
-  #pragma unroll
-  for (int m = 1; m < 16; m <<= 1)
-    #pragma unroll
-    for (int rr = 0; rr < 4; ++rr) { s[rr] += __shfl_xor(s[rr], m); q[rr] += __shfl_xor(q[rr], m); }
-  if (lr == 0)
-    #pragma unroll
-    for (int rr = 0; rr < 4; ++rr) {
-      ssum[lq * 4 + rr][wid] = s[rr];
-      ssq[lq * 4 + rr][wid] = q[rr];
-    }
-  __syncthreads();
-  float mu[4], rs[4];
-  #pragma unroll
-  for (int rr = 0; rr < 4; ++rr) {
-    int rl = lq * 4 + rr;
-    float sm = 0.f, sq = 0.f;
-    #pragma unroll
-    for (int w8 = 0; w8 < 8; ++w8) { sm += ssum[rl][w8]; sq += ssq[rl][w8]; }
-    float m_ = sm * (1.f / 256.f);
-    float var = sq * (1.f / 256.f) - m_ * m_;
-    mu[rr] = m_; rs[rr] = rsqrtf(var + 1e-5f);
-  }
+      int rl = ti * 16 + lq * 4 + rr;
+      float sm = 0.f, sq = 0.f;
+      #pragma unroll
+      for (int w8 = 0; w8 < 8; ++w8) { sm += ssum[rl][w8]; sq += ssq[rl][w8]; }
+      float m_ = sm * (1.f / 256.f);
+      float var = sq * (1.f / 256.f) - m_ * m_;
+      mu[ti][rr] = m_; rs[ti][rr] = rsqrtf(var + 1e-5f);
+    }
   #pragma unroll
   for (int t = 0; t < 2; ++t) {
     int col = cw + t * 16 + lr;
     float g = gamma[col], be = beta[col];
     #pragma unroll
-    for (int rr = 0; rr < 4; ++rr) {
-      int rl = lq * 4 + rr;
-      size_t idx = (size_t)(m0 + rl) * 256 + col;
-      float v = (acc[t][rr] - mu[rr]) * rs[rr] * g + be;
-      outf[idx] = v;
-      short vb = f2bf(v);
-      outbf[idx] = vb;
-      float po = prev[idx];
-      oqbf[idx] = f2bf(v + po);
-      prev[idx] = v;
-      if (SCORES) hid[rl][col] = vb;
-    }
+    for (int ti = 0; ti < 2; ++ti)
+      #pragma unroll
+      for (int rr = 0; rr < 4; ++rr) {
+        int rl = ti * 16 + lq * 4 + rr;
+        size_t idx = (size_t)(m0 + rl) * 256 + col;
+        float v = (acc[ti][t][rr] - mu[ti][rr]) * rs[ti][rr] * g + be;
+        outf[idx] = v;
+        short vb = f2bf(v);
+        outbf[idx] = vb;
+        float po = prev[idx];
+        oqbf[idx] = f2bf(v + po);
+        prev[idx] = v;
+        if (SCORES) hid[rl][col] = vb;
+      }
   }
   if (SCORES) {
     __syncthreads();
-    f32x4 sacc = (f32x4){0.f, 0.f, 0.f, 0.f};
+    f32x4 sacc[2];
+    sacc[0] = (f32x4){0.f, 0.f, 0.f, 0.f};
+    sacc[1] = (f32x4){0.f, 0.f, 0.f, 0.f};
     int trow = (wid < 5) ? wid * 16 + lr : 0;
     #pragma unroll 2
     for (int k0 = 0; k0 < 256; k0 += 32) {
-      bf16x8 a = *(const bf16x8*)&hid[lr][k0 + lq * 8];
+      bf16x8 a0 = *(const bf16x8*)&hid[lr][k0 + lq * 8];
+      bf16x8 a1 = *(const bf16x8*)&hid[16 + lr][k0 + lq * 8];
       bf16x8 w = *(const bf16x8*)(SCt + (size_t)trow * 256 + k0 + lq * 8);
-      sacc = __builtin_amdgcn_mfma_f32_16x16x32_bf16(a, w, sacc, 0, 0, 0);
+      sacc[0] = __builtin_amdgcn_mfma_f32_16x16x32_bf16(a0, w, sacc[0], 0, 0, 0);
+      sacc[1] = __builtin_amdgcn_mfma_f32_16x16x32_bf16(a1, w, sacc[1], 0, 0, 0);
     }
     if (wid < 5) {
       int col = wid * 16 + lr;
       float bv = scb[col];
       #pragma unroll
-      for (int rr = 0; rr < 4; ++rr)
-        scoresOut[(size_t)(m0 + lq * 4 + rr) * 80 + col] = sacc[rr] + bv;
+      for (int ti = 0; ti < 2; ++ti)
+        #pragma unroll
+        for (int rr = 0; rr < 4; ++rr)
+          scoresOut[(size_t)(m0 + ti * 16 + lq * 4 + rr) * 80 + col] = sacc[ti][rr] + bv;
     }
   }
 }
@@ -430,15 +502,15 @@
                            const float* __restrict__ scores, const float* __restrict__ lw1,
                            const float* __restrict__ lb1, const float* __restrict__ lw2,
                            const float* __restrict__ lb2, float* __restrict__ outp) {
-  __shared__ short h1[16][264];
-  __shared__ short h2[16][264];
-  __shared__ float cor[16][132];
-  __shared__ float dstl[16][4];
+  __shared__ short h1[32][264];
+  __shared__ short h2[32][264];
+  __shared__ float cor[32][132];
+  __shared__ float dstl[32][4];
   __shared__ float projs[33];
-  __shared__ float statl[16][20];
-  __shared__ float interb[16][4];
-  __shared__ float lqes[16];
-  const int m0 = blockIdx.x * 16;
+  __shared__ float statl[32][20];
+  __shared__ float interb[32][4];
+  __shared__ float lqes[32];
+  const int m0 = blockIdx.x * 32;
   const int tid = threadIdx.x, wid = tid >> 6, lane = tid & 63;
   const int lr = lane & 15, lq = lane >> 4;
   if (tid < 33) {
@@ -451,16 +523,20 @@
     projs[tid] = v;
   }
   {
-    f32x4 acc[2];
-    acc[0] = (f32x4){0.f, 0.f, 0.f, 0.f};
-    acc[1] = (f32x4){0.f, 0.f, 0.f, 0.f};
+    f32x4 acc[2][2];
+    #pragma unroll
+    for (int ti = 0; ti < 2; ++ti)
+      #pragma unroll
+      for (int t = 0; t < 2; ++t) acc[ti][t] = (f32x4){0.f, 0.f, 0.f, 0.f};
     #pragma unroll 2
     for (int k0 = 0; k0 < 256; k0 += 32) {
-      bf16x8 a = *(const bf16x8*)(A + (size_t)(m0 + lr) * 256 + k0 + lq * 8);
+      bf16x8 a0 = *(const bf16x8*)(A + (size_t)(m0 + lr) * 256 + k0 + lq * 8);
+      bf16x8 a1 = *(const bf16x8*)(A + (size_t)(m0 + 16 + lr) * 256 + k0 + lq * 8);
       #pragma unroll
       for (int t = 0; t < 2; ++t) {
         bf16x8 w = *(const bf16x8*)(W1t + (size_t)(wid * 32 + t * 16 + lr) * 256 + k0 + lq * 8);
-        acc[t] = __builtin_amdgcn_mfma_f32_16x16x32_bf16(a, w, acc[t], 0, 0, 0);
+        acc[0][t] = __builtin_amdgcn_mfma_f32_16x16x32_bf16(a0, w, acc[0][t], 0, 0, 0);
+        acc[1][t] = __builtin_amdgcn_mfma_f32_16x16x32_bf16(a1, w, acc[1][t], 0, 0, 0);
       }
     }
     #pragma unroll
@@ -468,25 +544,31 @@
       int col = wid * 32 + t * 16 + lr;
       float bv = b1[col];
       #pragma unroll
-      for (int rr = 0; rr < 4; ++rr) {
-        float v = acc[t][rr] + bv;
-        v = v / (1.f + __expf(-v));
-        h1[lq * 4 + rr][col] = f2bf(v);
-      }
+      for (int ti = 0; ti < 2; ++ti)
+        #pragma unroll
+        for (int rr = 0; rr < 4; ++rr) {
+          float v = acc[ti][t][rr] + bv;
+          v = v / (1.f + __expf(-v));
+          h1[ti * 16 + lq * 4 + rr][col] = f2bf(v);
+        }
     }
   }
   __syncthreads();
   {
-    f32x4 acc[2];
-    acc[0] = (f32x4){0.f, 0.f, 0.f, 0.f};
-    acc[1] = (f32x4){0.f, 0.f, 0.f, 0.f};
+    f32x4 acc[2][2];
+    #pragma unroll
+    for (int ti = 0; ti < 2; ++ti)
+      #pragma unroll
+      for (int t = 0; t < 2; ++t) acc[ti][t] = (f32x4){0.f, 0.f, 0.f, 0.f};
     #pragma unroll 2
     for (int k0 = 0; k0 < 256; k0 += 32) {
-      bf16x8 a = *(const bf16x8*)&h1[lr][k0 + lq * 8];
+      bf16x8 a0 = *(const bf16x8*)&h1[lr][k0 + lq * 8];
+      bf16x8 a1 = *(const bf16x8*)&h1[16 + lr][k0 + lq * 8];
       #pragma unroll
       for (int t = 0; t < 2; ++t) {
         bf16x8 w = *(const bf16x8*)(W2t + (size_t)(wid * 32 + t * 16 + lr) * 256 + k0 + lq * 8);
-        acc[t] = __builtin_amdgcn_mfma_f32_16x16x32_bf16(a, w, acc[t], 0, 0, 0);
+        acc[0][t] = __builtin_amdgcn_mfma_f32_16x16x32_bf16(a0, w, acc[0][t], 0, 0, 0);
+        acc[1][t] = __builtin_amdgcn_mfma_f32_16x16x32_bf16(a1, w, acc[1][t], 0, 0, 0);
       }
     }
     #pragma unroll
@@ -494,30 +576,35 @@
       int col = wid * 32 + t * 16 + lr;
       float bv = b2[col];
       #pragma unroll
-      for (int rr = 0; rr < 4; ++rr) {
-        float v = acc[t][rr] + bv;
-        v = v / (1.f + __expf(-v));
-        h2[lq * 4 + rr][col] = f2bf(v);
-      }
+      for (int ti = 0; ti < 2; ++ti)
+        #pragma unroll
+        for (int rr = 0; rr < 4; ++rr) {
+          float v = acc[ti][t][rr] + bv;
+          v = v / (1.f + __expf(-v));
+          h2[ti * 16 + lq * 4 + rr][col] = f2bf(v);
+        }
     }
   }
   __syncthreads();
   {
-    f32x4 acc[2];
+    f32x4 acc[2][2];
     int col[2], wr[2];
     #pragma unroll
     for (int j = 0; j < 2; ++j) {
-      acc[j] = (f32x4){0.f, 0.f, 0.f, 0.f};
+      acc[0][j] = (f32x4){0.f, 0.f, 0.f, 0.f};
+      acc[1][j] = (f32x4){0.f, 0.f, 0.f, 0.f};
       col[j] = (wid + j * 8) * 16 + lr;
       wr[j] = (col[j] < 132) ? col[j] : 0;
     }
     #pragma unroll 2
     for (int k0 = 0; k0 < 256; k0 += 32) {
-      bf16x8 a = *(const bf16x8*)&h2[lr][k0 + lq * 8];
+      bf16x8 a0 = *(const bf16x8*)&h2[lr][k0 + lq * 8];
+      bf16x8 a1 = *(const bf16x8*)&h2[16 + lr][k0 + lq * 8];
       #pragma unroll
       for (int j = 0; j < 2; ++j) {
         bf16x8 w = *(const bf16x8*)(W3t + (size_t)wr[j] * 256 + k0 + lq * 8);
-        acc[j] = __builtin_amdgcn_mfma_f32_16x16x32_bf16(a, w, acc[j], 0, 0, 0);
+        acc[0][j] = __builtin_amdgcn_mfma_f32_16x16x32_bf16(a0, w, acc[0][j], 0, 0, 0);
+        acc[1][j] = __builtin_amdgcn_mfma_f32_16x16x32_bf16(a1, w, acc[1][j], 0, 0, 0);
       }
     }
     #pragma unroll
@@ -525,16 +612,18 @@
       if (col[j] >= 132) continue;
       float bv = b3[col[j]];
       #pragma unroll
-      for (int rr = 0; rr < 4; ++rr) {
-        int rl = lq * 4 + rr, g = m0 + rl;
-        float v = acc[j][rr] + bv + cprev[(size_t)g * 132 + col[j]];
-        ccur[(size_t)g * 132 + col[j]] = v;
-        cor[rl][col[j]] = v;
-      }
-    }
-  }
-  __syncthreads();
-  if (tid < 64) {
+      for (int ti = 0; ti < 2; ++ti)
+        #pragma unroll
+        for (int rr = 0; rr < 4; ++rr) {
+          int rl = ti * 16 + lq * 4 + rr, g = m0 + rl;
+          float v = acc[ti][j][rr] + bv + cprev[(size_t)g * 132 + col[j]];
+          ccur[(size_t)g * 132 + col[j]] = v;
+          cor[rl][col[j]] = v;
+        }
+    }
+  }
+  __syncthreads();
+  if (tid < 128) {
     int r = tid >> 2, sd = tid & 3;
     const float* cp = &cor[r][sd * 33];
     float m = -1e30f;
@@ -563,7 +652,7 @@
     }
   }
   __syncthreads();
-  if (tid < 16) {
+  if (tid < 32) {
     int g = m0 + tid;
     float px = refi[g * 4], py = refi[g * 4 + 1];
     float qw = refi[g * 4 + 2] * 0.25f, qh = refi[g * 4 + 3] * 0.25f;
@@ -575,8 +664,8 @@
   }
   if (LQE) {
     #pragma unroll
-    for (int it = 0; it < 2; ++it) {
-      int row = wid * 2 + it;
+    for (int it = 0; it < 4; ++it) {
+      int row = wid * 4 + it;
       float sv = lb1[lane];
       #pragma unroll
       for (int i = 0; i < 20; ++i) sv += statl[row][i] * lw1[i * 64 + lane];
@@ -587,7 +676,7 @@
       if (lane == 0) lqes[row] = v + lb2[0];
     }
     __syncthreads();
-    for (int idx = tid; idx < 16 * 84; idx += 512) {
+    for (int idx = tid; idx < 32 * 84; idx += 512) {
       int r = idx / 84, c = idx - r * 84;
       int g = m0 + r;
       outp[(size_t)g * 84 + c] = (c < 4) ? interb[r][c]
@@ -602,22 +691,26 @@
                          const short* __restrict__ W2t, const float* __restrict__ b2,
                          const short* __restrict__ W3t, const float* __restrict__ b3,
                          const float* __restrict__ refc, float* __restrict__ refinit) {
-  __shared__ short h1[16][264];
-  __shared__ short h2[16][264];
-  const int m0 = blockIdx.x * 16;
+  __shared__ short h1[32][264];
+  __shared__ short h2[32][264];
+  const int m0 = blockIdx.x * 32;
   const int tid = threadIdx.x, wid = tid >> 6, lane = tid & 63;
   const int lr = lane & 15, lq = lane >> 4;
   {
-    f32x4 acc[2];
-    acc[0] = (f32x4){0.f, 0.f, 0.f, 0.f};
-    acc[1] = (f32x4){0.f, 0.f, 0.f, 0.f};
+    f32x4 acc[2][2];
+    #pragma unroll
+    for (int ti = 0; ti < 2; ++ti)
+      #pragma unroll
+      for (int t = 0; t < 2; ++t) acc[ti][t] = (f32x4){0.f, 0.f, 0.f, 0.f};
     #pragma unroll 2
     for (int k0 = 0; k0 < 256; k0 += 32) {
-      bf16x8 a = *(const bf16x8*)(A + (size_t)(m0 + lr) * 256 + k0 + lq * 8);
+      bf16x8 a0 = *(const bf16x8*)(A + (size_t)(m0 + lr) * 256 + k0 + lq * 8);
+      bf16x8 a1 = *(const bf16x8*)(A + (size_t)(m0 + 16 + lr) * 256 + k0 + lq * 8);
       #pragma unroll
       for (int t = 0; t < 2; ++t) {
         bf16x8 w = *(const bf16x8*)(W1t + (size_t)(wid * 32 + t * 16 + lr) * 256 + k0 + lq * 8);
-        acc[t] = __builtin_amdgcn_mfma_f32_16x16x32_bf16(a, w, acc[t], 0, 0, 0);
+        acc[0][t] = __builtin_amdgcn_mfma_f32_16x16x32_bf16(a0, w, acc[0][t], 0, 0, 0);
+        acc[1][t] = __builtin_amdgcn_mfma_f32_16x16x32_bf16(a1, w, acc[1][t], 0, 0, 0);
       }
     }
     #pragma unroll
@@ -625,25 +718,31 @@
       int col = wid * 32 + t * 16 + lr;
       float bv = b1[col];
       #pragma unroll
-      for (int rr = 0; rr < 4; ++rr) {
-        float v = acc[t][rr] + bv;
-        v = v / (1.f + __expf(-v));
-        h1[lq * 4 + rr][col] = f2bf(v);
-      }
+      for (int ti = 0; ti < 2; ++ti)
+        #pragma unroll
+        for (int rr = 0; rr < 4; ++rr) {
+          float v = acc[ti][t][rr] + bv;
+          v = v / (1.f + __expf(-v));
+          h1[ti * 16 + lq * 4 + rr][col] = f2bf(v);
+        }
     }
   }
   __syncthreads();
   {
-    f32x4 acc[2];
-    acc[0] = (f32x4){0.f, 0.f, 0.f, 0.f};
-    acc[1] = (f32x4){0.f, 0.f, 0.f, 0.f};
+    f32x4 acc[2][2];
+    #pragma unroll
+    for (int ti = 0; ti < 2; ++ti)
+      #pragma unroll
+      for (int t = 0; t < 2; ++t) acc[ti][t] = (f32x4){0.f, 0.f, 0.f, 0.f};
     #pragma unroll 2
     for (int k0 = 0; k0 < 256; k0 += 32) {
-      bf16x8 a = *(const bf16x8*)&h1[lr][k0 + lq * 8];
+      bf16x8 a0 = *(const bf16x8*)&h1[lr][k0 + lq * 8];
+      bf16x8 a1 = *(const bf16x8*)&h1[16 + lr][k0 + lq * 8];
       #pragma unroll
       for (int t = 0; t < 2; ++t) {
         bf16x8 w = *(const bf16x8*)(W2t + (size_t)(wid * 32 + t * 16 + lr) * 256 + k0 + lq * 8);
-        acc[t] = __builtin_amdgcn_mfma_f32_16x16x32_bf16(a, w, acc[t], 0, 0, 0);
+        acc[0][t] = __builtin_amdgcn_mfma_f32_16x16x32_bf16(a0, w, acc[0][t], 0, 0, 0);
+        acc[1][t] = __builtin_amdgcn_mfma_f32_16x16x32_bf16(a1, w, acc[1][t], 0, 0, 0);
       }
     }
     #pragma unroll
@@ -651,20 +750,23 @@
       int col = wid * 32 + t * 16 + lr;
       float bv = b2[col];
       #pragma unroll
-      for (int rr = 0; rr < 4; ++rr) {
-        float v = acc[t][rr] + bv;
-        v = v / (1.f + __expf(-v));
-        h2[lq * 4 + rr][col] = f2bf(v);
-      }
-    }
-  }
-  __syncthreads();
-  if (wid == 0) {
+      for (int ti = 0; ti < 2; ++ti)
+        #pragma unroll
+        for (int rr = 0; rr < 4; ++rr) {
+          float v = acc[ti][t][rr] + bv;
+          v = v / (1.f + __expf(-v));
+          h2[ti * 16 + lq * 4 + rr][col] = f2bf(v);
+        }
+    }
+  }
+  __syncthreads();
+  if (wid < 2) {
+    const int rbase = wid * 16;
     f32x4 acc = (f32x4){0.f, 0.f, 0.f, 0.f};
     const short* wp = W3t + (size_t)((lr < 4) ? lr : 0) * 256;
     #pragma unroll 2
     for (int k0 = 0; k0 < 256; k0 += 32) {
-      bf16x8 a = *(const bf16x8*)&h2[lr][k0 + lq * 8];
+      bf16x8 a = *(const bf16x8*)&h2[rbase + lr][k0 + lq * 8];
       bf16x8 w = *(const bf16x8*)(wp + k0 + lq * 8);
       acc = __builtin_amdgcn_mfma_f32_16x16x32_bf16(a, w, acc, 0, 0, 0);
     }
@@ -672,7 +774,7 @@
       float bv = b3[lr];
       #pragma unroll
       for (int rr = 0; rr < 4; ++rr) {
-        int g = m0 + lq * 4 + rr;
+        int g = m0 + rbase + lq * 4 + rr;
         float pre = acc[rr] + bv;
         float x = fminf(fmaxf(refc[(size_t)g * 4 + lr], 1e-5f), 1.f - 1e-5f);
         float is = logf(x) - log1pf(-x);
@@ -688,23 +790,26 @@
                         const float* __restrict__ t2,
                         const float* __restrict__ gamma, const float* __restrict__ beta,
                         float* __restrict__ output, short* __restrict__ outbf) {
-  __shared__ float sg[16][520];
-  const int m0 = blockIdx.x * 16;
+  __shared__ float sg[32][520];
+  const int m0 = blockIdx.x * 32;
   const int tid = threadIdx.x, wid = tid >> 6, lane = tid & 63;
   const int lr = lane & 15, lq = lane >> 4;
-  const int arow = m0 + lr;
-  f32x4 acc[4];
-  #pragma unroll
-  for (int t = 0; t < 4; ++t) acc[t] = (f32x4){0.f, 0.f, 0.f, 0.f};
+  f32x4 acc[2][4];
+  #pragma unroll
+  for (int ti = 0; ti < 2; ++ti)
+    #pragma unroll
+    for (int t = 0; t < 4; ++t) acc[ti][t] = (f32x4){0.f, 0.f, 0.f, 0.f};
   #pragma unroll 2
   for (int k0 = 0; k0 < 512; k0 += 32) {
     const short* src = (k0 < 256) ? Abf : tbf;
     int ko = (k0 < 256) ? k0 : k0 - 256;
-    bf16x8 a = *(const bf16x8*)(src + (size_t)arow * 256 + ko + lq * 8);
+    bf16x8 a0 = *(const bf16x8*)(src + (size_t)(m0 + lr) * 256 + ko + lq * 8);
+    bf16x8 a1 = *(const bf16x8*)(src + (size_t)(m0 + 16 + lr) * 256 + ko + lq * 8);
     #pragma unroll
     for (int t = 0; t < 4; ++t) {
       bf16x8 w = *(const bf16x8*)(Wt + (size_t)(wid * 64 + t * 16 + lr) * 512 + k0 + lq * 8);
-      acc[t] = __builtin_amdgcn_mfma_f32_16x16x32_bf16(a, w, acc[t], 0, 0, 0);
+      acc[0][t] = __builtin_amdgcn_mfma_f32_16x16x32_bf16(a0, w, acc[0][t], 0, 0, 0);
+      acc[1][t] = __builtin_amdgcn_mfma_f32_16x16x32_bf16(a1, w, acc[1][t], 0, 0, 0);
     }
   }
   #pragma unroll
@@ -712,14 +817,16 @@
     int col = wid * 64 + t * 16 + lr;
     float bv = bias[col];
     #pragma unroll
-    for (int rr = 0; rr < 4; ++rr) {
-      int rl = lq * 4 + rr;
-      sg[rl][col] = 1.f / (1.f + __expf(-(acc[t][rr] + bv)));
-    }
-  }
-  __syncthreads();
-  #pragma unroll
-  for (int it = 0; it < 2; ++it) {
+    for (int ti = 0; ti < 2; ++ti)
+      #pragma unroll
+      for (int rr = 0; rr < 4; ++rr) {
+        int rl = ti * 16 + lq * 4 + rr;
+        sg[rl][col] = 1.f / (1.f + __expf(-(acc[ti][t][rr] + bv)));
+      }
+  }
+  __syncthreads();
+  #pragma unroll
+  for (int it = 0; it < 4; ++it) {
     int rl = wid + it * 8;
     int rowg = m0 + rl;
     int c = lane * 4;
@@ -838,15 +945,17 @@
 }
 
 template<int BF16MEM>
-__launch_bounds__(256)
+__launch_bounds__(512)
 __global__ void deform_kernel(const void* __restrict__ memv, const float* __restrict__ offaw,
                               const float* __restrict__ refp,
                               float* __restrict__ t2, short* __restrict__ t2bf) {
   const int bi = blockIdx.x;
-  const int row = (bi & 7) * 600 + (bi >> 3);
+  const int tid = threadIdx.x;
+  const int sub = tid >> 8;
+  const int row = (bi & 7) * 600 + (bi >> 3) * 2 + sub;
   const int b = row / LQ_;
-  const int tid = threadIdx.x;
-  const int h = tid >> 5, c = tid & 31;
+  const int it = tid & 255;
+  const int h = it >> 5, c = it & 31;
   const float rx = refp[row * 4 + 0], ry = refp[row * 4 + 1];
   const float rw = refp[row * 4 + 2], rh = refp[row * 4 + 3];
   const float* awp = offaw + (size_t)row * 288 + 192 + h * SUMP_;
@@ -1016,43 +1125,43 @@
       output, outbf, out_prev, c_prev, ref_cur, qkvb, offawb);
 
   for (int i = 0; i < NLAYERS_; ++i) {
-    qp_qkv<<<dim3(300), 512, 0, stream>>>(ref_cur, qp_w1, qp_b1, qp2t, qp_b2,
+    qp_qkv<<<dim3(150), 512, 0, stream>>>(ref_cur, qp_w1, qp_b1, qp2t, qp_b2,
                                           output, outbf,
                                           sqkvt + (size_t)i * 768 * 256,
                                           qkvb + (size_t)i * 768, qp, qkv);
     attn3_kernel<<<dim3(B_ * NH_ * 2), 256, 0, stream>>>(qkv, tbf);
-    sow_ln_off<<<dim3(300), 512, 0, stream>>>(
+    sow_ln_off<<<dim3(150), 512, 0, stream>>>(
         tbf, sowt + (size_t)i * 65536, sa_ob + (size_t)i * D_, output,
         n1_g + (size_t)i * D_, n1_b + (size_t)i * D_, qp,
         soffawt + (size_t)i * 288 * 256, offawb + (size_t)i * 288,
         output, outbf, offawf);
 
     if (bf16mem)
-      deform_kernel<1><<<dim3(R_), 256, 0, stream>>>(membf, offawf, ref_cur, t2, tbf);
+      deform_kernel<1><<<dim3(R_ / 2), 512, 0, stream>>>(membf, offawf, ref_cur, t2, tbf);
     else
-      deform_kernel<0><<<dim3(R_), 256, 0, stream>>>(memory, offawf, ref_cur, t2, tbf);
-
-    gate_ln<<<dim3(300), 512, 0, stream>>>(outbf, tbf, gatet + (size_t)i * 262144,
+      deform_kernel<0><<<dim3(R_ / 2), 512, 0, stream>>>(memory, offawf, ref_cur, t2, tbf);
+
+    gate_ln<<<dim3(150), 512, 0, stream>>>(outbf, tbf, gatet + (size_t)i * 262144,
                                            gate_b + (size_t)i * 512, t2,
                                            gn_g + (size_t)i * D_, gn_b + (size_t)i * D_,
                                            output, outbf);
 
     if (i < NLAYERS_ - 1)
-      ffn_ln<0><<<dim3(300), 512, 0, stream>>>(outbf, ff1t + (size_t)i * 262144,
+      ffn_ln<0><<<dim3(150), 512, 0, stream>>>(outbf, ff1t + (size_t)i * 262144,
           ff1_b + (size_t)i * FF_, ff2t + (size_t)i * 262144, ff2_b + (size_t)i * D_,
           output, n3_g + (size_t)i * D_, n3_b + (size_t)i * D_,
           out_prev, output, outbf, oqbf, nullptr, nullptr, nullptr);
     else
-      ffn_ln<1><<<dim3(300), 512, 0, stream>>>(outbf, ff1t + (size_t)i * 262144,
+      ffn_ln<1><<<dim3(150), 512, 0, stream>>>(outbf, ff1t + (size_t)i * 262144,
           ff1_b + (size_t)i * FF_, ff2t + (size_t)i * 262144, ff2_b + (size_t)i * D_,
           output, n3_g + (size_t)i * D_, n3_b + (size_t)i * D_,
           out_prev, output, outbf, oqbf, sct, sc_b + (size_t)5 * NC_, scores);
 
     if (i == 0)
-      pb_fused<<<dim3(300), 512, 0, stream>>>(outbf, pb1t, pb_b1, pb2t, pb_b2,
+      pb_fused<<<dim3(150), 512, 0, stream>>>(outbf, pb1t, pb_b1, pb2t, pb_b2,
                                               pb3t, pb_b3, ref_cur, ref_init);
     if (i < NLAYERS_ - 1) {
-      fdr_kernel<0><<<dim3(300), 512, 0, stream>>>(oqbf,
+      fdr_kernel<0><<<dim3(150), 512, 0, stream>>>(oqbf,
           bb1t + (size_t)i * 65536, bb_b1 + (size_t)i * D_,
           bb2t + (size_t)i * 65536, bb_b2 + (size_t)i * D_,
           bb3t + (size_t)i * 33792, bb_b3 + (size_t)i * 4 * NBIN_,
@@ -1061,7 +1170,7 @@
       std::swap(c_prev, c_cur);
       std::swap(ref_cur, ref_nxt);
     } else {
-      fdr_kernel<1><<<dim3(300), 512, 0, stream>>>(oqbf,
+      fdr_kernel<1><<<dim3(150), 512, 0, stream>>>(oqbf,
           bb1t + (size_t)i * 65536, bb_b1 + (size_t)i * D_,
           bb2t + (size_t)i * 65536, bb_b2 + (size_t)i * D_,
           bb3t + (size_t)i * 33792, bb_b3 + (size_t)i * 4 * NBIN_,
```
